# Performance work log

Hardware: AMD Instinct MI355X
Metric: run time of the kernel (lower is better)

## Reference

```python
import jax, jax.numpy as jnp
import numpy as np

B, N, K = 8, 2048, 100  # graphs per batch, nodes per graph, diffpool clusters


def _bn(x, g, b, eps=1e-5):
    # BatchNorm1d in training mode over all B*N nodes (biased variance)
    m = x.mean(axis=(0, 1))
    v = x.var(axis=(0, 1))
    return (x - m) * jax.lax.rsqrt(v + eps) * g + b


def _norm_adj(A):
    # PyG gcn_norm: add remaining self-loops (fill=1), D^-1/2 (A+I) D^-1/2
    n = A.shape[-1]
    d = jnp.diagonal(A, axis1=-2, axis2=-1)
    A_hat = A + jnp.where(d == 0, 1.0, 0.0)[..., :, None] * jnp.eye(n, dtype=A.dtype)
    deg = A_hat.sum(-1)
    dinv = jnp.where(deg > 0, 1.0 / jnp.sqrt(deg), 0.0)
    return dinv[..., :, None] * A_hat * dinv[..., None, :]


def _gcn(An, x, W, b):
    # GCNConv: propagate(x @ W) + bias, with pre-normalized adjacency
    return An @ (x @ W) + b


def _forward(x, adj, W_in, W3030, Wp13, b30, b100, Wfc_pool, bfc_pool,
             W1, b1, W2, b2, gamma30, beta30, gamma100, beta100):
    A_w = _norm_adj(adj)                               # weighted (edge_attr) adjacency
    A_b = _norm_adj((adj > 0).astype(adj.dtype))       # pool convs ignore edge_attr
    # feature branch
    x11 = _bn(_gcn(A_w, x, W_in[0], b30[0]), gamma30[0], beta30[0])
    x12 = _bn(_gcn(A_w, x11, W3030[0], b30[1]), gamma30[1], beta30[1])
    x13 = _bn(_gcn(A_w, x12, W3030[1], b30[2]), gamma30[2], beta30[2])
    x1_out = jnp.concatenate([x11, x12, x13], -1).max(axis=1)   # [B,90]
    # assignment branch
    s11 = _bn(_gcn(A_b, x, W_in[1], b30[3]), gamma30[3], beta30[3])
    s12 = _bn(_gcn(A_b, s11, W3030[2], b30[4]), gamma30[4], beta30[4])
    s13 = _bn(_gcn(A_b, s12, Wp13, b100), gamma100, beta100)
    s1 = jnp.concatenate([s11, s12, s13], -1) @ Wfc_pool + bfc_pool  # [B,N,K]
    # dense_diff_pool (link/entropy losses are unused by the forward output)
    s = jax.nn.softmax(s1, -1)
    p1_x = jnp.einsum('bnk,bnd->bkd', s, x13)          # s^T x  [B,K,30]
    p1_adj = jnp.einsum('bnk,bnl->bkl', s, adj @ s)    # s^T A s  [B,K,K]
    # second stage on pooled (dense, weighted) graph
    A2 = _norm_adj(p1_adj)
    x21 = _bn(_gcn(A2, p1_x, W3030[3], b30[5]), gamma30[5], beta30[5])
    x22 = _bn(_gcn(A2, x21, W3030[4], b30[6]), gamma30[6], beta30[6])
    x23 = _bn(_gcn(A2, x22, W3030[5], b30[7]), gamma30[7], beta30[7])
    x2_out = jnp.concatenate([x21, x22, x23], -1).max(axis=1)   # [B,90]
    h = jnp.concatenate([x1_out, x2_out], -1) @ W1 + b1
    return jax.nn.relu(h) @ W2 + b2                    # [B,6]


def setup_inputs():
    key = jax.random.key(0)
    ks = jax.random.split(key, 12)
    u = jax.random.uniform(ks[0], (B, N, N), dtype=jnp.float32)
    mask = jax.random.uniform(ks[1], (B, N, N)) < 0.05
    A = jnp.triu(u * mask, 1)
    adj = A + jnp.swapaxes(A, -1, -2)
    x = jax.random.normal(ks[2], (B, N, 3), dtype=jnp.float32)
    w = lambda k, s: jax.random.normal(k, s, dtype=jnp.float32) * 0.1
    return dict(
        x=x, adj=adj,
        W_in=w(ks[3], (2, 3, 30)),      # conv11, pool_conv11
        W3030=w(ks[4], (6, 30, 30)),    # conv12, conv13, pool_conv12, conv21..23
        Wp13=w(ks[5], (30, 100)),
        b30=jnp.zeros((8, 30), jnp.float32),
        b100=jnp.zeros((100,), jnp.float32),
        Wfc_pool=w(ks[6], (160, 100)), bfc_pool=jnp.zeros((100,), jnp.float32),
        W1=w(ks[7], (180, 50)), b1=jnp.zeros((50,), jnp.float32),
        W2=w(ks[8], (50, 6)), b2=jnp.zeros((6,), jnp.float32),
        gamma30=jnp.ones((8, 30), jnp.float32), beta30=jnp.zeros((8, 30), jnp.float32),
        gamma100=jnp.ones((100,), jnp.float32), beta100=jnp.zeros((100,), jnp.float32),
    )


def reference(x, adj, W_in, W3030, Wp13, b30, b100, Wfc_pool, bfc_pool,
              W1, b1, W2, b2, gamma30, beta30, gamma100, beta100):
    return _forward(x, adj, W_in, W3030, Wp13, b30, b100, Wfc_pool, bfc_pool,
                    W1, b1, W2, b2, gamma30, beta30, gamma100, beta100)
```

## Files before the change

kernel.cpp:

```cpp
#include <hip/hip_runtime.h>
#include <hip/hip_fp16.h>
#include <cstdint>
#include <cstddef>

#define BATCH 8
#define NN 2048
#define RTOT 16384
#define CAP 176

static constexpr size_t OF_B1W   = 0;
static constexpr size_t OF_B1B   = 3840;
static constexpr size_t OF_B2W   = 7680;
static constexpr size_t OF_B2B   = 11520;
static constexpr size_t OF_B3W   = 15360;
static constexpr size_t OF_B3B   = 15840;
static constexpr size_t OF_S2    = 17440;
static constexpr size_t OF_CNT   = 17620;
static constexpr size_t ZEND     = 17632;
static constexpr size_t OF_ELLV  = 17664;
static constexpr size_t OF_ELLC  = OF_ELLV + 2883584;
static constexpr size_t OF_ROWLEN= OF_ELLC + 1441792;
static constexpr size_t OF_DINVW = OF_ROWLEN + 16384;
static constexpr size_t OF_DINVB = OF_DINVW + 16384;
static constexpr size_t OF_HWB   = OF_DINVB + 16384;
static constexpr size_t OF_HW3   = OF_HWB + 524288;
static constexpr size_t OF_HB100 = OF_HW3 + 262144;
static constexpr size_t OF_ZW    = OF_HB100 + 851968;
static constexpr size_t OF_ZB    = OF_ZW + 524288;
static constexpr size_t OF_X11   = OF_ZB + 1703936;
static constexpr size_t OF_X12   = OF_X11 + 524288;
static constexpr size_t OF_X13   = OF_X12 + 524288;
static constexpr size_t OF_S11   = OF_X13 + 524288;
static constexpr size_t OF_S12   = OF_S11 + 524288;
static constexpr size_t OF_PARTMAX = OF_S12 + 524288;

#define FMA4(acc, s, h) { acc.x += (s)*(h).x; acc.y += (s)*(h).y; acc.z += (s)*(h).z; acc.w += (s)*(h).w; }

__device__ __forceinline__ unsigned short f2h(float f) {
  _Float16 h = (_Float16)f;
  return *(unsigned short*)&h;
}
__device__ __forceinline__ float h2f(unsigned short s) {
  _Float16 h = *(_Float16*)&s;
  return (float)h;
}
__device__ __forceinline__ float2 h2f2(unsigned int u) {
  __half2 h = *(__half2*)&u;
  return __half22float2(h);
}

struct __align__(8) us4 { unsigned short x, y, z, w; };

#define ACC8(g, wt) { \
  float2 f0=h2f2((g).x), f1=h2f2((g).y), f2=h2f2((g).z), f3=h2f2((g).w); \
  acc[0] += (wt)*f0.x; acc[1] += (wt)*f0.y; acc[2] += (wt)*f1.x; acc[3] += (wt)*f1.y; \
  acc[4] += (wt)*f2.x; acc[5] += (wt)*f2.y; acc[6] += (wt)*f3.x; acc[7] += (wt)*f3.y; }


__global__ __launch_bounds__(256) void k_build_ell(
    const float* __restrict__ adj, const float* __restrict__ x,
    const float* __restrict__ Win, float* __restrict__ ellv,
    unsigned short* __restrict__ ellc, int* __restrict__ rowlen,
    float* __restrict__ dinvw, float* __restrict__ dinvb,
    unsigned short* __restrict__ Hwb, float* __restrict__ zbase)
{
  int r = blockIdx.x;
  int t = threadIdx.x, lane = t & 63, wv = t >> 6;
  if (blockIdx.x < 69) {
    int zi = blockIdx.x * 256 + t;
    if (zi < (int)ZEND) zbase[zi] = 0.f;
  }
  const float* row = adj + (size_t)r * NN;
  __shared__ int wcnt[4];
  __shared__ float wsumA[4];
  __shared__ float dsh[2];
  float4 a = ((const float4*)row)[t];
  float4 b = ((const float4*)row)[256 + t];
  float vals[8] = {a.x, a.y, a.z, a.w, b.x, b.y, b.z, b.w};
  int cbase0 = t*4, cbase1 = 1024 + t*4;
  int cnt = 0; float sum = 0.f;
#pragma unroll
  for (int k = 0; k < 8; ++k) { sum += vals[k]; cnt += (vals[k] != 0.f) ? 1 : 0; }
  int pre = cnt;
#pragma unroll
  for (int o = 1; o < 64; o <<= 1) { int n = __shfl_up(pre, o); if (lane >= o) pre += n; }
  int excl = pre - cnt;
  int wtot = __shfl(pre, 63);
#pragma unroll
  for (int o = 32; o; o >>= 1) sum += __shfl_down(sum, o);
  if (lane == 0) { wcnt[wv] = wtot; wsumA[wv] = sum; }
  __syncthreads();
  int base = 0;
  for (int w = 0; w < wv; ++w) base += wcnt[w];
  int p = base + excl;
  size_t rb = (size_t)r * CAP;
#pragma unroll
  for (int k = 0; k < 8; ++k) {
    float v = vals[k];
    if (v != 0.f && p < CAP) {
      ellv[rb + p] = v;
      ellc[rb + p] = (unsigned short)((k < 4) ? (cbase0 + k) : (cbase1 + (k - 4)));
      ++p;
    }
  }
  if (t == 0) {
    int tot = wcnt[0] + wcnt[1] + wcnt[2] + wcnt[3];
    float ws = wsumA[0] + wsumA[1] + wsumA[2] + wsumA[3];
    int nnz = tot < CAP ? tot : CAP;
    int n = nnz;
    while ((n & 3) && n < CAP) { ellv[rb + n] = 0.f; ellc[rb + n] = 0; ++n; }
    rowlen[r] = n;
    float dw = rsqrtf(ws + 1.f), db = rsqrtf((float)nnz + 1.f);
    dinvw[r] = dw; dinvb[r] = db;
    dsh[0] = dw; dsh[1] = db;
  }
  __syncthreads();
  if (t < 64) {
    int c = t & 31, side = t >> 5;
    float v = 0.f;
    if (c < 30) {
      float x0 = x[r*3], x1 = x[r*3+1], x2 = x[r*3+2];
      const float* W = Win + side*90;
      v = (x0*W[c] + x1*W[30+c] + x2*W[60+c]) * dsh[side];
    }
    Hwb[(size_t)r*64 + t] = f2h(v);
  }
}

__global__ __launch_bounds__(256) void k_spmm_pair(
    const unsigned short* __restrict__ Hwb, const float* __restrict__ ellv,
    const unsigned short* __restrict__ ellc, const int* __restrict__ rowlen,
    const float* __restrict__ dinvw, const float* __restrict__ dinvb,
    float* __restrict__ Zw, float* __restrict__ Zb,
    float* __restrict__ bktW, float* __restrict__ bktB)
{
  __shared__ float zsW[32][32];
  __shared__ float zsB[32][32];
  int t = threadIdx.x;
  int gid = blockIdx.x * 256 + t;
  int row = gid >> 3, q = gid & 7;
  int side = q >> 2, sub = q & 3;
  int len = rowlen[row];
  const float4* ev = (const float4*)(ellv + (size_t)row * CAP);
  const uint2*  ec = (const uint2*) (ellc + (size_t)row * CAP);
  const uint4* HP = (const uint4*)(Hwb + (size_t)(row >> 11) * (NN*64));
  float acc[8] = {0,0,0,0,0,0,0,0};
  int nit = len >> 2;
  for (int i = 0; i < nit; ++i) {
    float4 v = ev[i];
    uint2 cc = ec[i];
    int c0 = cc.x & 0xffff, c1 = cc.x >> 16, c2 = cc.y & 0xffff, c3 = cc.y >> 16;
    uint4 g0 = HP[c0*8+q], g1 = HP[c1*8+q], g2 = HP[c2*8+q], g3 = HP[c3*8+q];
    float w0 = side ? (v.x>0.f?1.f:0.f) : v.x;
    float w1 = side ? (v.y>0.f?1.f:0.f) : v.y;
    float w2 = side ? (v.z>0.f?1.f:0.f) : v.z;
    float w3 = side ? (v.w>0.f?1.f:0.f) : v.w;
    ACC8(g0, w0); ACC8(g1, w1); ACC8(g2, w2); ACC8(g3, w3);
  }
  uint4 hs = HP[(row & (NN-1))*8 + q];
  ACC8(hs, 1.f);
  float d = side ? dinvb[row] : dinvw[row];
#pragma unroll
  for (int k = 0; k < 8; ++k) acc[k] *= d;
  float* Zp = (side ? Zb : Zw) + (size_t)row*32 + sub*8;
  float4 o0 = {acc[0],acc[1],acc[2],acc[3]}, o1 = {acc[4],acc[5],acc[6],acc[7]};
  ((float4*)Zp)[0] = o0; ((float4*)Zp)[1] = o1;
  int rowloc = t >> 3;
  float (*zs)[32] = side ? zsB : zsW;
#pragma unroll
  for (int k = 0; k < 8; ++k) zs[rowloc][sub*8+k] = acc[k];
  __syncthreads();
  int copy = blockIdx.x & 63;
  if (t < 30) {
    float s1 = 0.f, s2 = 0.f;
    for (int r = 0; r < 32; ++r) { float v = zsW[r][t]; s1 += v; s2 += v*v; }
    atomicAdd(&bktW[(t*64+copy)*2],   s1);
    atomicAdd(&bktW[(t*64+copy)*2+1], s2);
  } else if (t >= 64 && t < 94) {
    int c = t - 64;
    float s1 = 0.f, s2 = 0.f;
    for (int r = 0; r < 32; ++r) { float v = zsB[r][c]; s1 += v; s2 += v*v; }
    atomicAdd(&bktB[(c*64+copy)*2],   s1);
    atomicAdd(&bktB[(c*64+copy)*2+1], s2);
  }
}

__global__ __launch_bounds__(256) void k_spmm_l3(
    const unsigned short* __restrict__ Hw3, const unsigned short* __restrict__ Hb100,
    const float* __restrict__ ellv, const unsigned short* __restrict__ ellc,
    const int* __restrict__ rowlen, const float* __restrict__ dinvw,
    const float* __restrict__ dinvb, float* __restrict__ Zw, float* __restrict__ Zb,
    float* __restrict__ bktW3, float* __restrict__ bktB3)
{
  __shared__ float zs[64][32];
  __shared__ float st[200];
  int t = threadIdx.x;
  if (blockIdx.x < 256) {
    int gid = blockIdx.x * 256 + t;
    int row = gid >> 2, q = gid & 3;
    int len = rowlen[row];
    const float4* ev = (const float4*)(ellv + (size_t)row * CAP);
    const uint2*  ec = (const uint2*) (ellc + (size_t)row * CAP);
    const uint4* HP = (const uint4*)(Hw3 + (size_t)(row >> 11) * (NN*32));
    float acc[8] = {0,0,0,0,0,0,0,0};
    int nit = len >> 2;
    for (int i = 0; i < nit; ++i) {
      float4 v = ev[i];
      uint2 cc = ec[i];
      int c0 = cc.x & 0xffff, c1 = cc.x >> 16, c2 = cc.y & 0xffff, c3 = cc.y >> 16;
      uint4 g0 = HP[c0*4+q], g1 = HP[c1*4+q], g2 = HP[c2*4+q], g3 = HP[c3*4+q];
      ACC8(g0, v.x); ACC8(g1, v.y); ACC8(g2, v.z); ACC8(g3, v.w);
    }
    uint4 hs = HP[(row & (NN-1))*4 + q];
    ACC8(hs, 1.f);
    float d = dinvw[row];
#pragma unroll
    for (int k = 0; k < 8; ++k) acc[k] *= d;
    float* Zp = Zw + (size_t)row*32 + q*8;
    float4 o0 = {acc[0],acc[1],acc[2],acc[3]}, o1 = {acc[4],acc[5],acc[6],acc[7]};
    ((float4*)Zp)[0] = o0; ((float4*)Zp)[1] = o1;
    int rowloc = t >> 2;
#pragma unroll
    for (int k = 0; k < 8; ++k) zs[rowloc][q*8+k] = acc[k];
    __syncthreads();
    if (t < 30) {
      float s1 = 0.f, s2 = 0.f;
      for (int r = 0; r < 64; ++r) { float v = zs[r][t]; s1 += v; s2 += v*v; }
      int copy = blockIdx.x & 7;
      atomicAdd(&bktW3[(t*8+copy)*2],   s1);
      atomicAdd(&bktW3[(t*8+copy)*2+1], s2);
    }
  } else {
    int bid = blockIdx.x - 256;
    for (int i = t; i < 200; i += 256) st[i] = 0.f;
    __syncthreads();
    int gid = bid * 256 + t;
    int row = gid / 13, q = gid - row*13;
    int len = rowlen[row];
    const float4* ev = (const float4*)(ellv + (size_t)row * CAP);
    const uint2*  ec = (const uint2*) (ellc + (size_t)row * CAP);
    const uint4* HP = (const uint4*)(Hb100 + (size_t)(row >> 11) * ((size_t)NN*104));
    float acc[8] = {0,0,0,0,0,0,0,0};
    int nit = len >> 2;
    for (int i = 0; i < nit; ++i) {
      float4 v = ev[i];
      uint2 cc = ec[i];
      int c0 = cc.x & 0xffff, c1 = cc.x >> 16, c2 = cc.y & 0xffff, c3 = cc.y >> 16;
      uint4 g0 = HP[c0*13+q], g1 = HP[c1*13+q], g2 = HP[c2*13+q], g3 = HP[c3*13+q];
      float w0 = (v.x>0.f?1.f:0.f), w1 = (v.y>0.f?1.f:0.f);
      float w2 = (v.z>0.f?1.f:0.f), w3 = (v.w>0.f?1.f:0.f);
      ACC8(g0, w0); ACC8(g1, w1); ACC8(g2, w2); ACC8(g3, w3);
    }
    uint4 hs = HP[(row & (NN-1))*13 + q];
    ACC8(hs, 1.f);
    float d = dinvb[row];
#pragma unroll
    for (int k = 0; k < 8; ++k) acc[k] *= d;
    float* Zp = Zb + (size_t)row*104 + q*8;
    float4 o0 = {acc[0],acc[1],acc[2],acc[3]}, o1 = {acc[4],acc[5],acc[6],acc[7]};
    ((float4*)Zp)[0] = o0; ((float4*)Zp)[1] = o1;
    int c0 = q*8;
#pragma unroll
    for (int k = 0; k < 8; ++k) {
      int ch = c0 + k;
      if (ch < 100) { atomicAdd(&st[ch*2], acc[k]); atomicAdd(&st[ch*2+1], acc[k]*acc[k]); }
    }
    __syncthreads();
    int copy = bid & 7;
    for (int i = t; i < 200; i += 256)
      atomicAdd(&bktB3[((i>>1)*8 + copy)*2 + (i&1)], st[i]);
  }
}

template<int LEVEL>
__global__ __launch_bounds__(256) void k_apply_gemm(
    const float* __restrict__ Zw, const float* __restrict__ bktW,
    const float* __restrict__ gW, const float* __restrict__ beW,
    float* __restrict__ xst, const float* __restrict__ Ww,
    const float* __restrict__ dinvw,
    const float* __restrict__ Zb, const float* __restrict__ bktB,
    const float* __restrict__ gB, const float* __restrict__ beB,
    float* __restrict__ sst, const float* __restrict__ Wb,
    const float* __restrict__ dinvb,
    unsigned short* __restrict__ HwOut, unsigned short* __restrict__ HbOut)
{
  constexpr int NGB = (LEVEL == 1) ? 8 : 26;
  constexpr int OSTRIDEB = (LEVEL == 1) ? 32 : 104;
  constexpr int NG = 8 + NGB;
  __shared__ float WwL[30*32];
  __shared__ float WbL[30*OSTRIDEB];
  __shared__ float awL[60], abL[60];
  int t = threadIdx.x;
  if (t < 60) {
    int c = t % 30;
    bool isW = t < 30;
    const float4* p = (const float4*)((isW ? bktW : bktB) + c*128);
    float s1 = 0.f, s2 = 0.f;
#pragma unroll
    for (int k = 0; k < 32; ++k) { float4 v = p[k]; s1 += v.x + v.z; s2 += v.y + v.w; }
    float mean = s1/16384.f, var = s2/16384.f - mean*mean, inv = rsqrtf(var + 1e-5f);
    float aa = (isW ? gW : gB)[c]*inv;
    float* dst = isW ? awL : abL;
    dst[c] = aa; dst[30+c] = (isW ? beW : beB)[c] - mean*aa;
  }
  for (int idx = t; idx < 30*32; idx += 256) {
    int k = idx >> 5, c = idx & 31;
    WwL[idx] = (c < 30) ? Ww[k*30 + c] : 0.f;
  }
  if (LEVEL == 1) {
    for (int idx = t; idx < 30*32; idx += 256) {
      int k = idx >> 5, c = idx & 31;
      WbL[idx] = (c < 30) ? Wb[k*30 + c] : 0.f;
    }
  } else {
    for (int idx = t; idx < 30*OSTRIDEB; idx += 256) {
      int k = idx / OSTRIDEB, j = idx % OSTRIDEB;
      WbL[idx] = (j < 100) ? Wb[k*100 + j] : 0.f;
    }
  }
  __syncthreads();
  int gid = blockIdx.x * 256 + t;
  int row = gid / NG, g = gid % NG;
  if (g < 8) {
    const float4* Z4 = (const float4*)Zw + (size_t)row*8;
    float4 z4[8];
#pragma unroll
    for (int u = 0; u < 8; ++u) z4[u] = Z4[u];
    const float* z = (const float*)z4;
    float4 xv;
    int ch = 4*g;
    xv.x = (ch+0 < 30) ? awL[ch+0]*z[ch+0] + awL[30+ch+0] : 0.f;
    xv.y = (ch+1 < 30) ? awL[ch+1]*z[ch+1] + awL[30+ch+1] : 0.f;
    xv.z = (ch+2 < 30) ? awL[ch+2]*z[ch+2] + awL[30+ch+2] : 0.f;
    xv.w = (ch+3 < 30) ? awL[ch+3]*z[ch+3] + awL[30+ch+3] : 0.f;
    ((float4*)xst)[(size_t)row*8+g] = xv;
    float4 o = {0,0,0,0};
#pragma unroll
    for (int k = 0; k < 30; ++k) {
      float xk = awL[k]*z[k] + awL[30+k];
      float4 w = *(const float4*)(WwL + k*32 + 4*g);
      FMA4(o, xk, w);
    }
    float d = dinvw[row];
    us4 pv = { f2h(d*o.x), f2h(d*o.y), f2h(d*o.z), f2h(d*o.w) };
    unsigned short* dst = (LEVEL == 1) ? (HwOut + (size_t)row*64 + 4*g)
                                       : (HwOut + (size_t)row*32 + 4*g);
    *(us4*)dst = pv;
  } else {
    int gb = g - 8;
    const float4* Z4 = (const float4*)Zb + (size_t)row*8;
    float4 z4[8];
#pragma unroll
    for (int u = 0; u < 8; ++u) z4[u] = Z4[u];
    const float* z = (const float*)z4;
    if (gb < 8) {
      int ch = 4*gb;
      float4 sv;
      sv.x = (ch+0 < 30) ? abL[ch+0]*z[ch+0] + abL[30+ch+0] : 0.f;
      sv.y = (ch+1 < 30) ? abL[ch+1]*z[ch+1] + abL[30+ch+1] : 0.f;
      sv.z = (ch+2 < 30) ? abL[ch+2]*z[ch+2] + abL[30+ch+2] : 0.f;
      sv.w = (ch+3 < 30) ? abL[ch+3]*z[ch+3] + abL[30+ch+3] : 0.f;
      ((float4*)sst)[(size_t)row*8+gb] = sv;
    }
    float4 o = {0,0,0,0};
#pragma unroll
    for (int k = 0; k < 30; ++k) {
      float sk = abL[k]*z[k] + abL[30+k];
      float4 w = *(const float4*)(WbL + k*OSTRIDEB + 4*gb);
      FMA4(o, sk, w);
    }
    float d = dinvb[row];
    us4 pv = { f2h(d*o.x), f2h(d*o.y), f2h(d*o.z), f2h(d*o.w) };
    unsigned short* dst = (LEVEL == 1) ? (HbOut + (size_t)row*64 + 32 + 4*gb)
                                       : (HbOut + (size_t)row*104 + 4*gb);
    *(us4*)dst = pv;
  }
}

__global__ __launch_bounds__(256) void k_fcpool(
    const float* __restrict__ Zw3, const float* __restrict__ bktW3,
    const float* __restrict__ gW3, const float* __restrict__ beW3,
    const float* __restrict__ Zb3, const float* __restrict__ bktB3,
    const float* __restrict__ g100, const float* __restrict__ be100,
    const float* __restrict__ s11, const float* __restrict__ s12,
    const float* __restrict__ Wfc, const float* __restrict__ bfc,
    float* __restrict__ x13, unsigned short* __restrict__ S)
{
  __shared__ float shm[14240];
  __shared__ float aw3[60], ab3[200];
  float* feat = shm;
  float* Wl = shm + 10240;
  int t = threadIdx.x;
  int g0 = blockIdx.x * 64;
  if (t < 30) {
    const float4* p = (const float4*)(bktW3 + t*16);
    float s1 = 0.f, s2 = 0.f;
#pragma unroll
    for (int k = 0; k < 4; ++k) { float4 v = p[k]; s1 += v.x + v.z; s2 += v.y + v.w; }
    float mean = s1/16384.f, var = s2/16384.f - mean*mean, inv = rsqrtf(var + 1e-5f);
    float aa = gW3[t]*inv; aw3[t] = aa; aw3[30+t] = beW3[t] - mean*aa;
  } else if (t >= 64 && t < 164) {
    int c = t - 64;
    const float4* p = (const float4*)(bktB3 + c*16);
    float s1 = 0.f, s2 = 0.f;
#pragma unroll
    for (int k = 0; k < 4; ++k) { float4 v = p[k]; s1 += v.x + v.z; s2 += v.y + v.w; }
    float mean = s1/16384.f, var = s2/16384.f - mean*mean, inv = rsqrtf(var + 1e-5f);
    float aa = g100[c]*inv; ab3[c] = aa; ab3[100+c] = be100[c] - mean*aa;
  }
  __syncthreads();
  for (int idx = t; idx < 64*160; idx += 256) {
    int l = idx / 160, c = idx % 160;
    int g = g0 + l;
    float v;
    if (c < 30) v = s11[(size_t)g*32 + c];
    else if (c < 60) v = s12[(size_t)g*32 + (c-30)];
    else { int k = c - 60; v = ab3[k]*Zb3[(size_t)g*104 + k] + ab3[100 + k]; }
    feat[l*160 + c] = v;
  }
  for (int idx = t; idx < 64*32; idx += 256) {
    int l = idx >> 5, c = idx & 31;
    int g = g0 + l;
    x13[(size_t)g*32+c] = (c < 30) ? aw3[c]*Zw3[(size_t)g*32+c] + aw3[30+c] : 0.f;
  }
  int np = t >> 3, kg = t & 7;
  int n0 = np*2, n1 = np*2 + 1;
  int kbase = kg*12 + (kg < 4 ? kg : 4);
  int klen  = kg < 4 ? 13 : 12;
  float a0[13], a1[13];
#pragma unroll
  for (int j = 0; j < 13; ++j) { a0[j] = 0.f; a1[j] = 0.f; }
  for (int ch = 0; ch < 4; ++ch) {
    __syncthreads();
    for (int idx = t; idx < 4000; idx += 256) {
      int r = idx/100, j = idx%100;
      Wl[r*100 + j] = Wfc[(ch*40 + r)*100 + j];
    }
    __syncthreads();
    for (int kk = 0; kk < 40; ++kk) {
      float f0 = feat[n0*160 + ch*40+kk];
      float f1 = feat[n1*160 + ch*40+kk];
#pragma unroll
      for (int j = 0; j < 13; ++j) {
        if (j < klen) {
          float w = Wl[kk*100 + kbase + j];
          a0[j] += f0*w; a1[j] += f1*w;
        }
      }
    }
  }
  __syncthreads();
  float* sRow = shm;
  for (int j = 0; j < klen; ++j) {
    int k = kbase + j;
    sRow[n0*100 + k] = a0[j] + bfc[k];
    sRow[n1*100 + k] = a1[j] + bfc[k];
  }
  __syncthreads();
  int n = t >> 2, part = t & 3;
  int i0 = part*25;
  float m = -3.4e38f;
  for (int i = 0; i < 25; ++i) m = fmaxf(m, sRow[n*100 + i0 + i]);
  m = fmaxf(m, __shfl_xor(m, 1));
  m = fmaxf(m, __shfl_xor(m, 2));
  float ev[25]; float s = 0.f;
  for (int i = 0; i < 25; ++i) { float e = __expf(sRow[n*100 + i0 + i] - m); ev[i] = e; s += e; }
  s += __shfl_xor(s, 1);
  s += __shfl_xor(s, 2);
  float rinv = 1.f / s;
  for (int i = 0; i < 25; ++i) S[(size_t)(g0+n)*104 + i0 + i] = f2h(ev[i] * rinv);
  if (part == 3) {
    S[(size_t)(g0+n)*104 + 100] = 0; S[(size_t)(g0+n)*104 + 101] = 0;
    S[(size_t)(g0+n)*104 + 102] = 0; S[(size_t)(g0+n)*104 + 103] = 0;
  }
}

__global__ __launch_bounds__(256) void k_spmm_as(
    const unsigned short* __restrict__ S, const float* __restrict__ ellv,
    const unsigned short* __restrict__ ellc, const int* __restrict__ rowlen,
    float* __restrict__ Z)
{
  int t = threadIdx.x;
  int gid = blockIdx.x * 256 + t;
  int row = gid / 13, q = gid - row*13;
  int len = rowlen[row];
  const float4* ev = (const float4*)(ellv + (size_t)row * CAP);
  const uint2*  ec = (const uint2*) (ellc + (size_t)row * CAP);
  const uint4* HP = (const uint4*)(S + (size_t)(row >> 11) * ((size_t)NN*104));
  float acc[8] = {0,0,0,0,0,0,0,0};
  int nit = len >> 2;
  for (int i = 0; i < nit; ++i) {
    float4 v = ev[i];
    uint2 cc = ec[i];
    int c0 = cc.x & 0xffff, c1 = cc.x >> 16, c2 = cc.y & 0xffff, c3 = cc.y >> 16;
    uint4 g0 = HP[c0*13+q], g1 = HP[c1*13+q], g2 = HP[c2*13+q], g3 = HP[c3*13+q];
    ACC8(g0, v.x); ACC8(g1, v.y); ACC8(g2, v.z); ACC8(g3, v.w);
  }
  float* Zp = Z + (size_t)row*104 + q*8;
  float4 o0 = {acc[0],acc[1],acc[2],acc[3]}, o1 = {acc[4],acc[5],acc[6],acc[7]};
  ((float4*)Zp)[0] = o0; ((float4*)Zp)[1] = o1;
}

__global__ __launch_bounds__(256) void k_pool_part(
    const unsigned short* __restrict__ S, const float* __restrict__ x13,
    const float* __restrict__ As, const float* __restrict__ x11,
    const float* __restrict__ x12, float* __restrict__ pp, float* __restrict__ pm)
{
  __shared__ float sL[64][100];
  __shared__ float xL[64][132];
  __shared__ float red[256];
  int t = threadIdx.x;
  int b = blockIdx.x >> 3, chunk = blockIdx.x & 7;
  int g00 = b * 2048 + chunk * 256;
  int kt = t/10, dt = t%10;
  int k0 = kt*4, d0 = dt*13;
  float acc[4][13];
#pragma unroll
  for (int a = 0; a < 4; ++a)
#pragma unroll
    for (int j = 0; j < 13; ++j) acc[a][j] = 0.f;
  for (int tile = 0; tile < 4; ++tile) {
    int g0 = g00 + tile*64;
    __syncthreads();
    for (int idx = t; idx < 64*100; idx += 256) {
      int l = idx/100, k = idx%100;
      sL[l][k] = h2f(S[(size_t)(g0+l)*104 + k]);
    }
    for (int idx = t; idx < 64*130; idx += 256) {
      int l = idx/130, d = idx%130;
      xL[l][d] = d < 30 ? x13[(size_t)(g0+l)*32 + d] : As[(size_t)(g0+l)*104 + (d-30)];
    }
    __syncthreads();
    if (t < 250) {
      for (int kk = 0; kk < 64; ++kk) {
        float sv[4];
#pragma unroll
        for (int a = 0; a < 4; ++a) sv[a] = sL[kk][k0+a];
#pragma unroll
        for (int j = 0; j < 13; ++j) {
          float xv = xL[kk][d0+j];
#pragma unroll
          for (int a = 0; a < 4; ++a) acc[a][j] += sv[a]*xv;
        }
      }
    }
  }
  if (t < 250) {
    float* dst = pp + (size_t)blockIdx.x * 13000;
    for (int a = 0; a < 4; ++a)
      for (int j = 0; j < 13; ++j)
        dst[(k0+a)*130 + (d0+j)] = acc[a][j];
  }
  __syncthreads();
  {
    int c = t & 31, rg = t >> 5;
    const float* srcs[3] = {x11, x12, x13};
    for (int a = 0; a < 3; ++a) {
      const float* p = srcs[a] + (size_t)(g00+rg)*32 + c;
      float m = -3.4e38f;
      for (int it = 0; it < 32; ++it) m = fmaxf(m, p[it*256]);
      red[t] = m;
      __syncthreads();
      if (t < 30) {
        float mm = red[t];
        for (int g = 1; g < 8; ++g) mm = fmaxf(mm, red[g*32+t]);
        pm[(size_t)blockIdx.x*90 + a*30 + t] = mm;
      }
      __syncthreads();
    }
  }
}

__global__ __launch_bounds__(256) void k_s2fused(
    const float* __restrict__ pp, const float* __restrict__ partmax,
    const float* __restrict__ Wm,
    const float* __restrict__ g30,
    const float* __restrict__ be30,
    float* __restrict__ bktS2,
    int* __restrict__ cnt,
    const float* __restrict__ W1, const float* __restrict__ b1,
    const float* __restrict__ W2, const float* __restrict__ b2,
    float* __restrict__ out)
{
  __shared__ float A2f[10000];
  __shared__ float buf1[3000];
  __shared__ float buf2[3200];
  __shared__ float WL[960];
  __shared__ float dl[100];
  __shared__ float st1[30], st2[30];
  __shared__ float coef[60];
  __shared__ float x1L[90], x2L[90], hh[50];
  int b = blockIdx.x, t = threadIdx.x;
  for (int idx = t; idx < 13000; idx += 256) {
    float s = 0.f;
    for (int ch = 0; ch < 8; ++ch) s += pp[(size_t)(b*8 + ch)*13000 + idx];
    int k = idx/130, d = idx%130;
    if (d < 30) buf1[k*30 + d] = s;
    else A2f[k*100 + (d-30)] = s;
  }
  __syncthreads();
  if (t < 100 && A2f[t*101] == 0.f) A2f[t*101] = 1.f;
  __syncthreads();
  if (t < 100) {
    float s = 0.f;
    for (int j = 0; j < 100; ++j) s += A2f[t*100 + j];
    dl[t] = s > 0.f ? rsqrtf(s) : 0.f;
  }
  __syncthreads();
  for (int idx = t; idx < 10000; idx += 256) {
    int i = idx/100, j = idx%100;
    A2f[idx] = dl[i]*dl[j]*A2f[idx];
  }
  int rp = t >> 2, cg = t & 3;
  int i0 = rp*2, c0 = cg*8;
  bool act = (t < 200);
  for (int L = 0; L < 3; ++L) {
    if (t < 30) { st1[t] = 0.f; st2[t] = 0.f; }
    const float* W = Wm + L*900;
    for (int idx = t; idx < 960; idx += 256) {
      int k = idx >> 5, c = idx & 31;
      WL[idx] = (c < 30) ? W[k*30 + c] : 0.f;
    }
    __syncthreads();
    if (act) {
      float a0[8] = {0,0,0,0,0,0,0,0}, a1[8] = {0,0,0,0,0,0,0,0};
      for (int k = 0; k < 30; ++k) {
        float xx0 = buf1[i0*30 + k], xx1 = buf1[(i0+1)*30 + k];
        float4 w0 = *(const float4*)&WL[k*32 + c0];
        float4 w1 = *(const float4*)&WL[k*32 + c0 + 4];
        a0[0] += xx0*w0.x; a0[1] += xx0*w0.y; a0[2] += xx0*w0.z; a0[3] += xx0*w0.w;
        a0[4] += xx0*w1.x; a0[5] += xx0*w1.y; a0[6] += xx0*w1.z; a0[7] += xx0*w1.w;
        a1[0] += xx1*w0.x; a1[1] += xx1*w0.y; a1[2] += xx1*w0.z; a1[3] += xx1*w0.w;
        a1[4] += xx1*w1.x; a1[5] += xx1*w1.y; a1[6] += xx1*w1.z; a1[7] += xx1*w1.w;
      }
      float4 s00 = {a0[0],a0[1],a0[2],a0[3]}, s01 = {a0[4],a0[5],a0[6],a0[7]};
      float4 s10 = {a1[0],a1[1],a1[2],a1[3]}, s11v = {a1[4],a1[5],a1[6],a1[7]};
      *(float4*)&buf2[i0*32 + c0]       = s00;
      *(float4*)&buf2[i0*32 + c0 + 4]   = s01;
      *(float4*)&buf2[(i0+1)*32 + c0]   = s10;
      *(float4*)&buf2[(i0+1)*32 + c0+4] = s11v;
    }
    __syncthreads();
    if (act) {
      float z0[8] = {0,0,0,0,0,0,0,0}, z1[8] = {0,0,0,0,0,0,0,0};
      for (int j = 0; j < 100; ++j) {
        float av0 = A2f[i0*100 + j], av1 = A2f[(i0+1)*100 + j];
        float4 t0 = *(const float4*)&buf2[j*32 + c0];
        float4 t1 = *(const float4*)&buf2[j*32 + c0 + 4];
        z0[0] += av0*t0.x; z0[1] += av0*t0.y; z0[2] += av0*t0.z; z0[3] += av0*t0.w;
        z0[4] += av0*t1.x; z0[5] += av0*t1.y; z0[6] += av0*t1.z; z0[7] += av0*t1.w;
        z1[0] += av1*t0.x; z1[1] += av1*t0.y; z1[2] += av1*t0.z; z1[3] += av1*t0.w;
        z1[4] += av1*t1.x; z1[5] += av1*t1.y; z1[6] += av1*t1.z; z1[7] += av1*t1.w;
      }
#pragma unroll
      for (int k = 0; k < 8; ++k) {
        int c = c0 + k;
        if (c < 30) {
          buf1[i0*30 + c]     = z0[k];
          buf1[(i0+1)*30 + c] = z1[k];
          atomicAdd(&st1[c], z0[k] + z1[k]);
          atomicAdd(&st2[c], z0[k]*z0[k] + z1[k]*z1[k]);
        }
      }
    }
    __syncthreads();
    if (t < 30) {
      atomicAdd(&bktS2[(L*30+t)*2],   st1[t]);
      atomicAdd(&bktS2[(L*30+t)*2+1], st2[t]);
    }
    __syncthreads();
    if (t == 0) {
      __threadfence();
      atomicAdd(cnt, 1);
      while (atomicAdd(cnt, 0) < (L+1)*8) {}
      __threadfence();
    }
    __syncthreads();
    if (t < 30) {
      float s1 = atomicAdd(&bktS2[(L*30+t)*2],   0.f);
      float s2 = atomicAdd(&bktS2[(L*30+t)*2+1], 0.f);
      float mean = s1/800.f, var = s2/800.f - mean*mean, inv = rsqrtf(var + 1e-5f);
      float aa = g30[L*30+t]*inv;
      coef[t] = aa; coef[30+t] = be30[L*30+t] - mean*aa;
    }
    __syncthreads();
    if (L < 2) {
      for (int idx = t; idx < 3000; idx += 256) {
        int c = idx % 30;
        buf1[idx] = coef[c]*buf1[idx] + coef[30+c];
      }
      __syncthreads();
      if (t < 30) {
        float m = -3.4e38f;
        for (int i = 0; i < 100; ++i) m = fmaxf(m, buf1[i*30+t]);
        x2L[L*30+t] = m;
      }
      __syncthreads();
    } else {
      if (t < 30) {
        float m = -3.4e38f;
        for (int i = 0; i < 100; ++i) m = fmaxf(m, coef[t]*buf1[i*30+t] + coef[30+t]);
        x2L[60+t] = m;
      }
    }
  }
  if (t < 90) {
    float m = -3.4e38f;
    for (int s = 0; s < 8; ++s) m = fmaxf(m, partmax[(size_t)(b*8+s)*90 + t]);
    x1L[t] = m;
  }
  __syncthreads();
  if (t < 50) {
    float a = b1[t];
    for (int k = 0; k < 90; ++k) a += x1L[k]*W1[k*50+t];
    for (int k = 0; k < 90; ++k) a += x2L[k]*W1[(90+k)*50+t];
    hh[t] = fmaxf(a, 0.f);
  }
  __syncthreads();
  if (t < 6) {
    float a = b2[t];
    for (int j = 0; j < 50; ++j) a += hh[j]*W2[j*6+t];
    out[b*6+t] = a;
  }
}

extern "C" void kernel_launch(void* const* d_in, const int* in_sizes, int n_in,
                              void* d_out, int out_size, void* d_ws, size_t ws_size,
                              hipStream_t stream)
{
  const float* x    = (const float*)d_in[0];
  const float* adj  = (const float*)d_in[1];
  const float* Win  = (const float*)d_in[2];
  const float* W3030= (const float*)d_in[3];
  const float* Wp13 = (const float*)d_in[4];
  const float* Wfc  = (const float*)d_in[7];
  const float* bfc  = (const float*)d_in[8];
  const float* W1   = (const float*)d_in[9];
  const float* b1   = (const float*)d_in[10];
  const float* W2   = (const float*)d_in[11];
  const float* b2   = (const float*)d_in[12];
  const float* g30  = (const float*)d_in[13];
  const float* be30 = (const float*)d_in[14];
  const float* g100 = (const float*)d_in[15];
  const float* be100= (const float*)d_in[16];
  float* out = (float*)d_out;

  float* wsf = (float*)d_ws;
  float* bL1W = wsf + OF_B1W;  float* bL1B = wsf + OF_B1B;
  float* bL2W = wsf + OF_B2W;  float* bL2B = wsf + OF_B2B;
  float* bL3W = wsf + OF_B3W;  float* bL3B = wsf + OF_B3B;
  float* bktS2 = wsf + OF_S2;
  int*   cnt  = (int*)(wsf + OF_CNT);
  float* ellv  = wsf + OF_ELLV;
  unsigned short* ellc = (unsigned short*)(wsf + OF_ELLC);
  int*   rowlen = (int*)(wsf + OF_ROWLEN);
  float* dinvw = wsf + OF_DINVW;
  float* dinvb = wsf + OF_DINVB;
  unsigned short* Hwb   = (unsigned short*)(wsf + OF_HWB);
  unsigned short* Hw3   = (unsigned short*)(wsf + OF_HW3);
  unsigned short* Hb100 = (unsigned short*)(wsf + OF_HB100);
  unsigned short* S     = Hb100;
  float* Zw = wsf + OF_ZW;
  float* Zb = wsf + OF_ZB;
  float* x11 = wsf + OF_X11;
  float* x12 = wsf + OF_X12;
  float* x13 = wsf + OF_X13;
  float* s11 = wsf + OF_S11;
  float* s12 = wsf + OF_S12;
  float* pp  = wsf + OF_S11;
  float* partmax = wsf + OF_PARTMAX;

  k_build_ell<<<RTOT, 256, 0, stream>>>(adj, x, Win, ellv, ellc, rowlen, dinvw, dinvb, Hwb, wsf);

  k_spmm_pair<<<512, 256, 0, stream>>>(Hwb, ellv, ellc, rowlen, dinvw, dinvb, Zw, Zb, bL1W, bL1B);
  k_apply_gemm<1><<<1024, 256, 0, stream>>>(Zw, bL1W, g30+0, be30+0, x11, W3030+0, dinvw,
                                            Zb, bL1B, g30+90, be30+90, s11, W3030+2*900, dinvb, Hwb, Hwb);

  k_spmm_pair<<<512, 256, 0, stream>>>(Hwb, ellv, ellc, rowlen, dinvw, dinvb, Zw, Zb, bL2W, bL2B);
  k_apply_gemm<2><<<2176, 256, 0, stream>>>(Zw, bL2W, g30+30, be30+30, x12, W3030+900, dinvw,
                                            Zb, bL2B, g30+120, be30+120, s12, Wp13, dinvb, Hw3, Hb100);

  k_spmm_l3<<<1088, 256, 0, stream>>>(Hw3, Hb100, ellv, ellc, rowlen, dinvw, dinvb, Zw, Zb, bL3W, bL3B);
  k_fcpool<<<256, 256, 0, stream>>>(Zw, bL3W, g30+60, be30+60, Zb, bL3B, g100, be100,
                                    s11, s12, Wfc, bfc, x13, S);

  k_spmm_as<<<832, 256, 0, stream>>>(S, ellv, ellc, rowlen, Zb );
  k_pool_part<<<64, 256, 0, stream>>>(S, x13, Zb, x11, x12, pp, partmax);

  k_s2fused<<<BATCH, 256, 0, stream>>>(pp, partmax, W3030+3*900, g30+150, be30+150,
                                       bktS2, cnt, W1, b1, W2, b2, out);
}
```

Measured before the change: 655.8 us.

## Fuse all stages into one persistent kernel with software grid barriers

Replaces the sequence of nine kernel launches with a single persistent kernel of 512 blocks that steps through every stage and separates them with atomic-counter grid barriers. Intermediate buffers are given separate workspace regions so phases no longer alias each other, and the zeroing of the counters and accumulators moves to a hipMemsetAsync. The aim is to remove launch gaps and per-kernel tail effects. In exchange, each stage runs with a fixed grid and 256 threads per block, so occupancy and parallelism per stage change, the barriers spin on global atomics, and the large static shared array may limit how many blocks fit per CU. Correctness relies on all 512 blocks being resident at the same time.

```diff
diff --git a/kernel.cpp b/kernel.cpp
--- a/kernel.cpp
+++ b/kernel.cpp
@@ -7,6 +7,7 @@
 #define NN 2048
 #define RTOT 16384
 #define CAP 176
+#define NBLK 512
 
 static constexpr size_t OF_B1W   = 0;
 static constexpr size_t OF_B1B   = 3840;
@@ -22,17 +23,25 @@
 static constexpr size_t OF_ROWLEN= OF_ELLC + 1441792;
 static constexpr size_t OF_DINVW = OF_ROWLEN + 16384;
 static constexpr size_t OF_DINVB = OF_DINVW + 16384;
-static constexpr size_t OF_HWB   = OF_DINVB + 16384;
-static constexpr size_t OF_HW3   = OF_HWB + 524288;
+static constexpr size_t OF_HWB1  = OF_DINVB + 16384;
+static constexpr size_t OF_HWB2  = OF_HWB1 + 524288;
+static constexpr size_t OF_HW3   = OF_HWB2 + 524288;
 static constexpr size_t OF_HB100 = OF_HW3 + 262144;
-static constexpr size_t OF_ZW    = OF_HB100 + 851968;
-static constexpr size_t OF_ZB    = OF_ZW + 524288;
-static constexpr size_t OF_X11   = OF_ZB + 1703936;
+static constexpr size_t OF_S     = OF_HB100 + 851968;
+static constexpr size_t OF_ZWA   = OF_S + 851968;
+static constexpr size_t OF_ZBA   = OF_ZWA + 524288;
+static constexpr size_t OF_ZWB   = OF_ZBA + 524288;
+static constexpr size_t OF_ZBB   = OF_ZWB + 524288;
+static constexpr size_t OF_ZWC   = OF_ZBB + 524288;
+static constexpr size_t OF_ZBC   = OF_ZWC + 524288;
+static constexpr size_t OF_AS    = OF_ZBC + 1703936;
+static constexpr size_t OF_X11   = OF_AS + 1703936;
 static constexpr size_t OF_X12   = OF_X11 + 524288;
 static constexpr size_t OF_X13   = OF_X12 + 524288;
 static constexpr size_t OF_S11   = OF_X13 + 524288;
 static constexpr size_t OF_S12   = OF_S11 + 524288;
-static constexpr size_t OF_PARTMAX = OF_S12 + 524288;
+static constexpr size_t OF_PP    = OF_S12 + 524288;
+static constexpr size_t OF_PARTMAX = OF_PP + 832000;
 
 #define FMA4(acc, s, h) { acc.x += (s)*(h).x; acc.y += (s)*(h).y; acc.z += (s)*(h).z; acc.w += (s)*(h).w; }
 
@@ -56,88 +65,26 @@
   acc[0] += (wt)*f0.x; acc[1] += (wt)*f0.y; acc[2] += (wt)*f1.x; acc[3] += (wt)*f1.y; \
   acc[4] += (wt)*f2.x; acc[5] += (wt)*f2.y; acc[6] += (wt)*f3.x; acc[7] += (wt)*f3.y; }
 
-
-__global__ __launch_bounds__(256) void k_build_ell(
-    const float* __restrict__ adj, const float* __restrict__ x,
-    const float* __restrict__ Win, float* __restrict__ ellv,
-    unsigned short* __restrict__ ellc, int* __restrict__ rowlen,
-    float* __restrict__ dinvw, float* __restrict__ dinvb,
-    unsigned short* __restrict__ Hwb, float* __restrict__ zbase)
+__device__ __forceinline__ void gridbar(int* cnt, int target) {
+  __syncthreads();
+  if (threadIdx.x == 0) {
+    __threadfence();
+    atomicAdd(cnt, 1);
+    while (atomicAdd(cnt, 0) < target) {}
+    __threadfence();
+  }
+  __syncthreads();
+}
+
+__device__ __forceinline__ void spmm_pair_body(
+    int vb, int t, float* shm,
+    const unsigned short* Hwb, const float* ellv, const unsigned short* ellc,
+    const int* rowlen, const float* dinvw, const float* dinvb,
+    float* Zw, float* Zb, float* bktW, float* bktB)
 {
-  int r = blockIdx.x;
-  int t = threadIdx.x, lane = t & 63, wv = t >> 6;
-  if (blockIdx.x < 69) {
-    int zi = blockIdx.x * 256 + t;
-    if (zi < (int)ZEND) zbase[zi] = 0.f;
-  }
-  const float* row = adj + (size_t)r * NN;
-  __shared__ int wcnt[4];
-  __shared__ float wsumA[4];
-  __shared__ float dsh[2];
-  float4 a = ((const float4*)row)[t];
-  float4 b = ((const float4*)row)[256 + t];
-  float vals[8] = {a.x, a.y, a.z, a.w, b.x, b.y, b.z, b.w};
-  int cbase0 = t*4, cbase1 = 1024 + t*4;
-  int cnt = 0; float sum = 0.f;
-#pragma unroll
-  for (int k = 0; k < 8; ++k) { sum += vals[k]; cnt += (vals[k] != 0.f) ? 1 : 0; }
-  int pre = cnt;
-#pragma unroll
-  for (int o = 1; o < 64; o <<= 1) { int n = __shfl_up(pre, o); if (lane >= o) pre += n; }
-  int excl = pre - cnt;
-  int wtot = __shfl(pre, 63);
-#pragma unroll
-  for (int o = 32; o; o >>= 1) sum += __shfl_down(sum, o);
-  if (lane == 0) { wcnt[wv] = wtot; wsumA[wv] = sum; }
-  __syncthreads();
-  int base = 0;
-  for (int w = 0; w < wv; ++w) base += wcnt[w];
-  int p = base + excl;
-  size_t rb = (size_t)r * CAP;
-#pragma unroll
-  for (int k = 0; k < 8; ++k) {
-    float v = vals[k];
-    if (v != 0.f && p < CAP) {
-      ellv[rb + p] = v;
-      ellc[rb + p] = (unsigned short)((k < 4) ? (cbase0 + k) : (cbase1 + (k - 4)));
-      ++p;
-    }
-  }
-  if (t == 0) {
-    int tot = wcnt[0] + wcnt[1] + wcnt[2] + wcnt[3];
-    float ws = wsumA[0] + wsumA[1] + wsumA[2] + wsumA[3];
-    int nnz = tot < CAP ? tot : CAP;
-    int n = nnz;
-    while ((n & 3) && n < CAP) { ellv[rb + n] = 0.f; ellc[rb + n] = 0; ++n; }
-    rowlen[r] = n;
-    float dw = rsqrtf(ws + 1.f), db = rsqrtf((float)nnz + 1.f);
-    dinvw[r] = dw; dinvb[r] = db;
-    dsh[0] = dw; dsh[1] = db;
-  }
-  __syncthreads();
-  if (t < 64) {
-    int c = t & 31, side = t >> 5;
-    float v = 0.f;
-    if (c < 30) {
-      float x0 = x[r*3], x1 = x[r*3+1], x2 = x[r*3+2];
-      const float* W = Win + side*90;
-      v = (x0*W[c] + x1*W[30+c] + x2*W[60+c]) * dsh[side];
-    }
-    Hwb[(size_t)r*64 + t] = f2h(v);
-  }
-}
-
-__global__ __launch_bounds__(256) void k_spmm_pair(
-    const unsigned short* __restrict__ Hwb, const float* __restrict__ ellv,
-    const unsigned short* __restrict__ ellc, const int* __restrict__ rowlen,
-    const float* __restrict__ dinvw, const float* __restrict__ dinvb,
-    float* __restrict__ Zw, float* __restrict__ Zb,
-    float* __restrict__ bktW, float* __restrict__ bktB)
-{
-  __shared__ float zsW[32][32];
-  __shared__ float zsB[32][32];
-  int t = threadIdx.x;
-  int gid = blockIdx.x * 256 + t;
+  float* zsW = shm;
+  float* zsB = shm + 1024;
+  int gid = vb * 256 + t;
   int row = gid >> 3, q = gid & 7;
   int side = q >> 2, sub = q & 3;
   int len = rowlen[row];
@@ -166,80 +113,419 @@
   float4 o0 = {acc[0],acc[1],acc[2],acc[3]}, o1 = {acc[4],acc[5],acc[6],acc[7]};
   ((float4*)Zp)[0] = o0; ((float4*)Zp)[1] = o1;
   int rowloc = t >> 3;
-  float (*zs)[32] = side ? zsB : zsW;
-#pragma unroll
-  for (int k = 0; k < 8; ++k) zs[rowloc][sub*8+k] = acc[k];
+  float* zs = side ? zsB : zsW;
+#pragma unroll
+  for (int k = 0; k < 8; ++k) zs[rowloc*32 + sub*8+k] = acc[k];
   __syncthreads();
-  int copy = blockIdx.x & 63;
+  int copy = vb & 63;
   if (t < 30) {
     float s1 = 0.f, s2 = 0.f;
-    for (int r = 0; r < 32; ++r) { float v = zsW[r][t]; s1 += v; s2 += v*v; }
+    for (int r = 0; r < 32; ++r) { float v = zsW[r*32 + t]; s1 += v; s2 += v*v; }
     atomicAdd(&bktW[(t*64+copy)*2],   s1);
     atomicAdd(&bktW[(t*64+copy)*2+1], s2);
   } else if (t >= 64 && t < 94) {
     int c = t - 64;
     float s1 = 0.f, s2 = 0.f;
-    for (int r = 0; r < 32; ++r) { float v = zsB[r][c]; s1 += v; s2 += v*v; }
+    for (int r = 0; r < 32; ++r) { float v = zsB[r*32 + c]; s1 += v; s2 += v*v; }
     atomicAdd(&bktB[(c*64+copy)*2],   s1);
     atomicAdd(&bktB[(c*64+copy)*2+1], s2);
   }
 }
 
-__global__ __launch_bounds__(256) void k_spmm_l3(
-    const unsigned short* __restrict__ Hw3, const unsigned short* __restrict__ Hb100,
-    const float* __restrict__ ellv, const unsigned short* __restrict__ ellc,
-    const int* __restrict__ rowlen, const float* __restrict__ dinvw,
-    const float* __restrict__ dinvb, float* __restrict__ Zw, float* __restrict__ Zb,
-    float* __restrict__ bktW3, float* __restrict__ bktB3)
+template<int LEVEL>
+__device__ __forceinline__ void apply_phase(
+    int blk, int t, float* shm,
+    const float* Zw, const float* bktW, const float* gW, const float* beW,
+    float* xst, const float* Ww, const float* dinvw,
+    const float* Zb, const float* bktB, const float* gB, const float* beB,
+    float* sst, const float* Wb, const float* dinvb,
+    unsigned short* HwOut, unsigned short* HbOut)
 {
-  __shared__ float zs[64][32];
-  __shared__ float st[200];
-  int t = threadIdx.x;
-  if (blockIdx.x < 256) {
-    int gid = blockIdx.x * 256 + t;
-    int row = gid >> 2, q = gid & 3;
-    int len = rowlen[row];
-    const float4* ev = (const float4*)(ellv + (size_t)row * CAP);
-    const uint2*  ec = (const uint2*) (ellc + (size_t)row * CAP);
-    const uint4* HP = (const uint4*)(Hw3 + (size_t)(row >> 11) * (NN*32));
-    float acc[8] = {0,0,0,0,0,0,0,0};
-    int nit = len >> 2;
-    for (int i = 0; i < nit; ++i) {
-      float4 v = ev[i];
-      uint2 cc = ec[i];
-      int c0 = cc.x & 0xffff, c1 = cc.x >> 16, c2 = cc.y & 0xffff, c3 = cc.y >> 16;
-      uint4 g0 = HP[c0*4+q], g1 = HP[c1*4+q], g2 = HP[c2*4+q], g3 = HP[c3*4+q];
-      ACC8(g0, v.x); ACC8(g1, v.y); ACC8(g2, v.z); ACC8(g3, v.w);
-    }
-    uint4 hs = HP[(row & (NN-1))*4 + q];
-    ACC8(hs, 1.f);
-    float d = dinvw[row];
-#pragma unroll
-    for (int k = 0; k < 8; ++k) acc[k] *= d;
-    float* Zp = Zw + (size_t)row*32 + q*8;
-    float4 o0 = {acc[0],acc[1],acc[2],acc[3]}, o1 = {acc[4],acc[5],acc[6],acc[7]};
-    ((float4*)Zp)[0] = o0; ((float4*)Zp)[1] = o1;
-    int rowloc = t >> 2;
-#pragma unroll
-    for (int k = 0; k < 8; ++k) zs[rowloc][q*8+k] = acc[k];
-    __syncthreads();
+  constexpr int NGB = (LEVEL == 1) ? 8 : 26;
+  constexpr int OSTRIDEB = (LEVEL == 1) ? 32 : 104;
+  constexpr int NG = 8 + NGB;
+  constexpr int NVB = RTOT * NG / 256;
+  float* WwL = shm;
+  float* WbL = shm + 960;
+  float* awL = shm + 4080;
+  float* abL = shm + 4140;
+  if (t < 60) {
+    int c = t % 30;
+    bool isW = t < 30;
+    const float4* p = (const float4*)((isW ? bktW : bktB) + c*128);
+    float s1 = 0.f, s2 = 0.f;
+#pragma unroll
+    for (int k = 0; k < 32; ++k) { float4 v = p[k]; s1 += v.x + v.z; s2 += v.y + v.w; }
+    float mean = s1/16384.f, var = s2/16384.f - mean*mean, inv = rsqrtf(var + 1e-5f);
+    float aa = (isW ? gW : gB)[c]*inv;
+    float* dst = isW ? awL : abL;
+    dst[c] = aa; dst[30+c] = (isW ? beW : beB)[c] - mean*aa;
+  }
+  for (int idx = t; idx < 30*32; idx += 256) {
+    int k = idx >> 5, c = idx & 31;
+    WwL[idx] = (c < 30) ? Ww[k*30 + c] : 0.f;
+  }
+  if (LEVEL == 1) {
+    for (int idx = t; idx < 30*32; idx += 256) {
+      int k = idx >> 5, c = idx & 31;
+      WbL[idx] = (c < 30) ? Wb[k*30 + c] : 0.f;
+    }
+  } else {
+    for (int idx = t; idx < 30*OSTRIDEB; idx += 256) {
+      int k = idx / OSTRIDEB, j = idx % OSTRIDEB;
+      WbL[idx] = (j < 100) ? Wb[k*100 + j] : 0.f;
+    }
+  }
+  __syncthreads();
+  for (int vb = blk; vb < NVB; vb += NBLK) {
+    int gid = vb * 256 + t;
+    int row = gid / NG, g = gid % NG;
+    if (g < 8) {
+      const float4* Z4 = (const float4*)Zw + (size_t)row*8;
+      float4 z4[8];
+#pragma unroll
+      for (int u = 0; u < 8; ++u) z4[u] = Z4[u];
+      const float* z = (const float*)z4;
+      float4 xv;
+      int ch = 4*g;
+      xv.x = (ch+0 < 30) ? awL[ch+0]*z[ch+0] + awL[30+ch+0] : 0.f;
+      xv.y = (ch+1 < 30) ? awL[ch+1]*z[ch+1] + awL[30+ch+1] : 0.f;
+      xv.z = (ch+2 < 30) ? awL[ch+2]*z[ch+2] + awL[30+ch+2] : 0.f;
+      xv.w = (ch+3 < 30) ? awL[ch+3]*z[ch+3] + awL[30+ch+3] : 0.f;
+      ((float4*)xst)[(size_t)row*8+g] = xv;
+      float4 o = {0,0,0,0};
+#pragma unroll
+      for (int k = 0; k < 30; ++k) {
+        float xk = awL[k]*z[k] + awL[30+k];
+        float4 w = *(const float4*)(WwL + k*32 + 4*g);
+        FMA4(o, xk, w);
+      }
+      float d = dinvw[row];
+      us4 pv = { f2h(d*o.x), f2h(d*o.y), f2h(d*o.z), f2h(d*o.w) };
+      unsigned short* dst = (LEVEL == 1) ? (HwOut + (size_t)row*64 + 4*g)
+                                         : (HwOut + (size_t)row*32 + 4*g);
+      *(us4*)dst = pv;
+    } else {
+      int gb = g - 8;
+      const float4* Z4 = (const float4*)Zb + (size_t)row*8;
+      float4 z4[8];
+#pragma unroll
+      for (int u = 0; u < 8; ++u) z4[u] = Z4[u];
+      const float* z = (const float*)z4;
+      if (gb < 8) {
+        int ch = 4*gb;
+        float4 sv;
+        sv.x = (ch+0 < 30) ? abL[ch+0]*z[ch+0] + abL[30+ch+0] : 0.f;
+        sv.y = (ch+1 < 30) ? abL[ch+1]*z[ch+1] + abL[30+ch+1] : 0.f;
+        sv.z = (ch+2 < 30) ? abL[ch+2]*z[ch+2] + abL[30+ch+2] : 0.f;
+        sv.w = (ch+3 < 30) ? abL[ch+3]*z[ch+3] + abL[30+ch+3] : 0.f;
+        ((float4*)sst)[(size_t)row*8+gb] = sv;
+      }
+      float4 o = {0,0,0,0};
+#pragma unroll
+      for (int k = 0; k < 30; ++k) {
+        float sk = abL[k]*z[k] + abL[30+k];
+        float4 w = *(const float4*)(WbL + k*OSTRIDEB + 4*gb);
+        FMA4(o, sk, w);
+      }
+      float d = dinvb[row];
+      us4 pv = { f2h(d*o.x), f2h(d*o.y), f2h(d*o.z), f2h(d*o.w) };
+      unsigned short* dst = (LEVEL == 1) ? (HbOut + (size_t)row*64 + 32 + 4*gb)
+                                         : (HbOut + (size_t)row*104 + 4*gb);
+      *(us4*)dst = pv;
+    }
+  }
+}
+
+__global__ __launch_bounds__(256) void k_mega(
+    const float* adj, const float* x, const float* Win, const float* W3030,
+    const float* Wp13, const float* Wfc, const float* bfc,
+    const float* W1, const float* b1, const float* W2, const float* b2,
+    const float* g30, const float* be30, const float* g100, const float* be100,
+    float* wsf, float* out)
+{
+  __shared__ float shm[17664];
+  const int blk = blockIdx.x, t = threadIdx.x;
+  int* cnt  = (int*)(wsf + OF_CNT);
+  int* cnt2 = cnt + 1;
+  float* ellv = wsf + OF_ELLV;
+  unsigned short* ellc = (unsigned short*)(wsf + OF_ELLC);
+  int* rowlen = (int*)(wsf + OF_ROWLEN);
+  float* dinvw = wsf + OF_DINVW;
+  float* dinvb = wsf + OF_DINVB;
+  unsigned short* Hwb1 = (unsigned short*)(wsf + OF_HWB1);
+  unsigned short* Hwb2 = (unsigned short*)(wsf + OF_HWB2);
+  unsigned short* Hw3  = (unsigned short*)(wsf + OF_HW3);
+  unsigned short* Hb100= (unsigned short*)(wsf + OF_HB100);
+  unsigned short* S    = (unsigned short*)(wsf + OF_S);
+  float* ZwA = wsf + OF_ZWA;  float* ZbA = wsf + OF_ZBA;
+  float* ZwB = wsf + OF_ZWB;  float* ZbB = wsf + OF_ZBB;
+  float* ZwC = wsf + OF_ZWC;  float* ZbC = wsf + OF_ZBC;
+  float* As  = wsf + OF_AS;
+  float* x11 = wsf + OF_X11;  float* x12 = wsf + OF_X12;  float* x13 = wsf + OF_X13;
+  float* s11 = wsf + OF_S11;  float* s12 = wsf + OF_S12;
+  float* pp  = wsf + OF_PP;   float* partmax = wsf + OF_PARTMAX;
+  float* bL1W = wsf + OF_B1W;  float* bL1B = wsf + OF_B1B;
+  float* bL2W = wsf + OF_B2W;  float* bL2B = wsf + OF_B2B;
+  float* bL3W = wsf + OF_B3W;  float* bL3B = wsf + OF_B3B;
+  float* bktS2 = wsf + OF_S2;
+
+  {
+    int* wcnt = (int*)shm;
+    float* wsumA = shm + 4;
+    float* dsh = shm + 8;
+    int lane = t & 63, wv = t >> 6;
+    for (int r = blk; r < RTOT; r += NBLK) {
+      __syncthreads();
+      const float* row = adj + (size_t)r * NN;
+      float4 a = ((const float4*)row)[t];
+      float4 b = ((const float4*)row)[256 + t];
+      float vals[8] = {a.x, a.y, a.z, a.w, b.x, b.y, b.z, b.w};
+      int cbase0 = t*4, cbase1 = 1024 + t*4;
+      int cnt_ = 0; float sum = 0.f;
+#pragma unroll
+      for (int k = 0; k < 8; ++k) { sum += vals[k]; cnt_ += (vals[k] != 0.f) ? 1 : 0; }
+      int pre = cnt_;
+#pragma unroll
+      for (int o = 1; o < 64; o <<= 1) { int n = __shfl_up(pre, o); if (lane >= o) pre += n; }
+      int excl = pre - cnt_;
+      int wtot = __shfl(pre, 63);
+#pragma unroll
+      for (int o = 32; o; o >>= 1) sum += __shfl_down(sum, o);
+      if (lane == 0) { wcnt[wv] = wtot; wsumA[wv] = sum; }
+      __syncthreads();
+      int base = 0;
+      for (int w = 0; w < wv; ++w) base += wcnt[w];
+      int p = base + excl;
+      size_t rb = (size_t)r * CAP;
+#pragma unroll
+      for (int k = 0; k < 8; ++k) {
+        float v = vals[k];
+        if (v != 0.f && p < CAP) {
+          ellv[rb + p] = v;
+          ellc[rb + p] = (unsigned short)((k < 4) ? (cbase0 + k) : (cbase1 + (k - 4)));
+          ++p;
+        }
+      }
+      if (t == 0) {
+        int tot = wcnt[0] + wcnt[1] + wcnt[2] + wcnt[3];
+        float ws = wsumA[0] + wsumA[1] + wsumA[2] + wsumA[3];
+        int nnz = tot < CAP ? tot : CAP;
+        int n = nnz;
+        while ((n & 3) && n < CAP) { ellv[rb + n] = 0.f; ellc[rb + n] = 0; ++n; }
+        rowlen[r] = n;
+        float dw = rsqrtf(ws + 1.f), db = rsqrtf((float)nnz + 1.f);
+        dinvw[r] = dw; dinvb[r] = db;
+        dsh[0] = dw; dsh[1] = db;
+      }
+      __syncthreads();
+      if (t < 64) {
+        int c = t & 31, side = t >> 5;
+        float v = 0.f;
+        if (c < 30) {
+          float x0 = x[r*3], x1 = x[r*3+1], x2 = x[r*3+2];
+          const float* W = Win + side*90;
+          v = (x0*W[c] + x1*W[30+c] + x2*W[60+c]) * dsh[side];
+        }
+        Hwb1[(size_t)r*64 + t] = f2h(v);
+      }
+    }
+  }
+  gridbar(cnt, 1*NBLK);
+
+  spmm_pair_body(blk, t, shm, Hwb1, ellv, ellc, rowlen, dinvw, dinvb, ZwA, ZbA, bL1W, bL1B);
+  gridbar(cnt, 2*NBLK);
+
+  apply_phase<1>(blk, t, shm, ZwA, bL1W, g30+0, be30+0, x11, W3030+0, dinvw,
+                 ZbA, bL1B, g30+90, be30+90, s11, W3030+2*900, dinvb, Hwb2, Hwb2);
+  gridbar(cnt, 3*NBLK);
+
+  spmm_pair_body(blk, t, shm, Hwb2, ellv, ellc, rowlen, dinvw, dinvb, ZwB, ZbB, bL2W, bL2B);
+  gridbar(cnt, 4*NBLK);
+
+  apply_phase<2>(blk, t, shm, ZwB, bL2W, g30+30, be30+30, x12, W3030+900, dinvw,
+                 ZbB, bL2B, g30+120, be30+120, s12, Wp13, dinvb, Hw3, Hb100);
+  gridbar(cnt, 5*NBLK);
+
+  for (int vb = blk; vb < 1088; vb += NBLK) {
+    __syncthreads();
+    if (vb < 256) {
+      float* zs = shm;
+      int gid = vb * 256 + t;
+      int row = gid >> 2, q = gid & 3;
+      int len = rowlen[row];
+      const float4* ev = (const float4*)(ellv + (size_t)row * CAP);
+      const uint2*  ec = (const uint2*) (ellc + (size_t)row * CAP);
+      const uint4* HP = (const uint4*)(Hw3 + (size_t)(row >> 11) * (NN*32));
+      float acc[8] = {0,0,0,0,0,0,0,0};
+      int nit = len >> 2;
+      for (int i = 0; i < nit; ++i) {
+        float4 v = ev[i];
+        uint2 cc = ec[i];
+        int c0 = cc.x & 0xffff, c1 = cc.x >> 16, c2 = cc.y & 0xffff, c3 = cc.y >> 16;
+        uint4 g0 = HP[c0*4+q], g1 = HP[c1*4+q], g2 = HP[c2*4+q], g3 = HP[c3*4+q];
+        ACC8(g0, v.x); ACC8(g1, v.y); ACC8(g2, v.z); ACC8(g3, v.w);
+      }
+      uint4 hs = HP[(row & (NN-1))*4 + q];
+      ACC8(hs, 1.f);
+      float d = dinvw[row];
+#pragma unroll
+      for (int k = 0; k < 8; ++k) acc[k] *= d;
+      float* Zp = ZwC + (size_t)row*32 + q*8;
+      float4 o0 = {acc[0],acc[1],acc[2],acc[3]}, o1 = {acc[4],acc[5],acc[6],acc[7]};
+      ((float4*)Zp)[0] = o0; ((float4*)Zp)[1] = o1;
+      int rowloc = t >> 2;
+#pragma unroll
+      for (int k = 0; k < 8; ++k) zs[rowloc*32 + q*8+k] = acc[k];
+      __syncthreads();
+      if (t < 30) {
+        float s1 = 0.f, s2 = 0.f;
+        for (int r = 0; r < 64; ++r) { float v = zs[r*32 + t]; s1 += v; s2 += v*v; }
+        int copy = vb & 7;
+        atomicAdd(&bL3W[(t*8+copy)*2],   s1);
+        atomicAdd(&bL3W[(t*8+copy)*2+1], s2);
+      }
+    } else {
+      float* st = shm + 2048;
+      int bid = vb - 256;
+      for (int i = t; i < 200; i += 256) st[i] = 0.f;
+      __syncthreads();
+      int gid = bid * 256 + t;
+      int row = gid / 13, q = gid - row*13;
+      int len = rowlen[row];
+      const float4* ev = (const float4*)(ellv + (size_t)row * CAP);
+      const uint2*  ec = (const uint2*) (ellc + (size_t)row * CAP);
+      const uint4* HP = (const uint4*)(Hb100 + (size_t)(row >> 11) * ((size_t)NN*104));
+      float acc[8] = {0,0,0,0,0,0,0,0};
+      int nit = len >> 2;
+      for (int i = 0; i < nit; ++i) {
+        float4 v = ev[i];
+        uint2 cc = ec[i];
+        int c0 = cc.x & 0xffff, c1 = cc.x >> 16, c2 = cc.y & 0xffff, c3 = cc.y >> 16;
+        uint4 g0 = HP[c0*13+q], g1 = HP[c1*13+q], g2 = HP[c2*13+q], g3 = HP[c3*13+q];
+        float w0 = (v.x>0.f?1.f:0.f), w1 = (v.y>0.f?1.f:0.f);
+        float w2 = (v.z>0.f?1.f:0.f), w3 = (v.w>0.f?1.f:0.f);
+        ACC8(g0, w0); ACC8(g1, w1); ACC8(g2, w2); ACC8(g3, w3);
+      }
+      uint4 hs = HP[(row & (NN-1))*13 + q];
+      ACC8(hs, 1.f);
+      float d = dinvb[row];
+#pragma unroll
+      for (int k = 0; k < 8; ++k) acc[k] *= d;
+      float* Zp = ZbC + (size_t)row*104 + q*8;
+      float4 o0 = {acc[0],acc[1],acc[2],acc[3]}, o1 = {acc[4],acc[5],acc[6],acc[7]};
+      ((float4*)Zp)[0] = o0; ((float4*)Zp)[1] = o1;
+      int c0 = q*8;
+#pragma unroll
+      for (int k = 0; k < 8; ++k) {
+        int ch = c0 + k;
+        if (ch < 100) { atomicAdd(&st[ch*2], acc[k]); atomicAdd(&st[ch*2+1], acc[k]*acc[k]); }
+      }
+      __syncthreads();
+      int copy = bid & 7;
+      for (int i = t; i < 200; i += 256)
+        atomicAdd(&bL3B[((i>>1)*8 + copy)*2 + (i&1)], st[i]);
+    }
+  }
+  gridbar(cnt, 6*NBLK);
+
+  if (blk < 256) {
+    float* feat = shm;
+    float* Wl = shm + 10240;
+    float* aw3 = shm + 14240;
+    float* ab3 = shm + 14300;
+    int g0 = blk * 64;
     if (t < 30) {
+      const float4* p = (const float4*)(bL3W + t*16);
       float s1 = 0.f, s2 = 0.f;
-      for (int r = 0; r < 64; ++r) { float v = zs[r][t]; s1 += v; s2 += v*v; }
-      int copy = blockIdx.x & 7;
-      atomicAdd(&bktW3[(t*8+copy)*2],   s1);
-      atomicAdd(&bktW3[(t*8+copy)*2+1], s2);
-    }
-  } else {
-    int bid = blockIdx.x - 256;
-    for (int i = t; i < 200; i += 256) st[i] = 0.f;
-    __syncthreads();
-    int gid = bid * 256 + t;
+#pragma unroll
+      for (int k = 0; k < 4; ++k) { float4 v = p[k]; s1 += v.x + v.z; s2 += v.y + v.w; }
+      float mean = s1/16384.f, var = s2/16384.f - mean*mean, inv = rsqrtf(var + 1e-5f);
+      float aa = g30[60+t]*inv; aw3[t] = aa; aw3[30+t] = be30[60+t] - mean*aa;
+    } else if (t >= 64 && t < 164) {
+      int c = t - 64;
+      const float4* p = (const float4*)(bL3B + c*16);
+      float s1 = 0.f, s2 = 0.f;
+#pragma unroll
+      for (int k = 0; k < 4; ++k) { float4 v = p[k]; s1 += v.x + v.z; s2 += v.y + v.w; }
+      float mean = s1/16384.f, var = s2/16384.f - mean*mean, inv = rsqrtf(var + 1e-5f);
+      float aa = g100[c]*inv; ab3[c] = aa; ab3[100+c] = be100[c] - mean*aa;
+    }
+    __syncthreads();
+    for (int idx = t; idx < 64*160; idx += 256) {
+      int l = idx / 160, c = idx % 160;
+      int g = g0 + l;
+      float v;
+      if (c < 30) v = s11[(size_t)g*32 + c];
+      else if (c < 60) v = s12[(size_t)g*32 + (c-30)];
+      else { int k = c - 60; v = ab3[k]*ZbC[(size_t)g*104 + k] + ab3[100 + k]; }
+      feat[l*160 + c] = v;
+    }
+    for (int idx = t; idx < 64*32; idx += 256) {
+      int l = idx >> 5, c = idx & 31;
+      int g = g0 + l;
+      x13[(size_t)g*32+c] = (c < 30) ? aw3[c]*ZwC[(size_t)g*32+c] + aw3[30+c] : 0.f;
+    }
+    int np = t >> 3, kg = t & 7;
+    int n0 = np*2, n1 = np*2 + 1;
+    int kbase = kg*12 + (kg < 4 ? kg : 4);
+    int klen  = kg < 4 ? 13 : 12;
+    float a0[13], a1[13];
+#pragma unroll
+    for (int j = 0; j < 13; ++j) { a0[j] = 0.f; a1[j] = 0.f; }
+    for (int ch = 0; ch < 4; ++ch) {
+      __syncthreads();
+      for (int idx = t; idx < 4000; idx += 256) {
+        int r = idx/100, j = idx%100;
+        Wl[r*100 + j] = Wfc[(ch*40 + r)*100 + j];
+      }
+      __syncthreads();
+      for (int kk = 0; kk < 40; ++kk) {
+        float f0 = feat[n0*160 + ch*40+kk];
+        float f1 = feat[n1*160 + ch*40+kk];
+#pragma unroll
+        for (int j = 0; j < 13; ++j) {
+          if (j < klen) {
+            float w = Wl[kk*100 + kbase + j];
+            a0[j] += f0*w; a1[j] += f1*w;
+          }
+        }
+      }
+    }
+    __syncthreads();
+    float* sRow = shm;
+    for (int j = 0; j < klen; ++j) {
+      int k = kbase + j;
+      sRow[n0*100 + k] = a0[j] + bfc[k];
+      sRow[n1*100 + k] = a1[j] + bfc[k];
+    }
+    __syncthreads();
+    int n = t >> 2, part = t & 3;
+    int i0 = part*25;
+    float m = -3.4e38f;
+    for (int i = 0; i < 25; ++i) m = fmaxf(m, sRow[n*100 + i0 + i]);
+    m = fmaxf(m, __shfl_xor(m, 1));
+    m = fmaxf(m, __shfl_xor(m, 2));
+    float ev[25]; float s = 0.f;
+    for (int i = 0; i < 25; ++i) { float e = __expf(sRow[n*100 + i0 + i] - m); ev[i] = e; s += e; }
+    s += __shfl_xor(s, 1);
+    s += __shfl_xor(s, 2);
+    float rinv = 1.f / s;
+    for (int i = 0; i < 25; ++i) S[(size_t)(g0+n)*104 + i0 + i] = f2h(ev[i] * rinv);
+    if (part == 3) {
+      S[(size_t)(g0+n)*104 + 100] = 0; S[(size_t)(g0+n)*104 + 101] = 0;
+      S[(size_t)(g0+n)*104 + 102] = 0; S[(size_t)(g0+n)*104 + 103] = 0;
+    }
+  }
+  gridbar(cnt, 7*NBLK);
+
+  for (int vb = blk; vb < 832; vb += NBLK) {
+    int gid = vb * 256 + t;
     int row = gid / 13, q = gid - row*13;
     int len = rowlen[row];
     const float4* ev = (const float4*)(ellv + (size_t)row * CAP);
     const uint2*  ec = (const uint2*) (ellc + (size_t)row * CAP);
-    const uint4* HP = (const uint4*)(Hb100 + (size_t)(row >> 11) * ((size_t)NN*104));
+    const uint4* HP = (const uint4*)(S + (size_t)(row >> 11) * ((size_t)NN*104));
     float acc[8] = {0,0,0,0,0,0,0,0};
     int nit = len >> 2;
     for (int i = 0; i < nit; ++i) {
@@ -247,480 +533,227 @@
       uint2 cc = ec[i];
       int c0 = cc.x & 0xffff, c1 = cc.x >> 16, c2 = cc.y & 0xffff, c3 = cc.y >> 16;
       uint4 g0 = HP[c0*13+q], g1 = HP[c1*13+q], g2 = HP[c2*13+q], g3 = HP[c3*13+q];
-      float w0 = (v.x>0.f?1.f:0.f), w1 = (v.y>0.f?1.f:0.f);
-      float w2 = (v.z>0.f?1.f:0.f), w3 = (v.w>0.f?1.f:0.f);
-      ACC8(g0, w0); ACC8(g1, w1); ACC8(g2, w2); ACC8(g3, w3);
-    }
-    uint4 hs = HP[(row & (NN-1))*13 + q];
-    ACC8(hs, 1.f);
-    float d = dinvb[row];
-#pragma unroll
-    for (int k = 0; k < 8; ++k) acc[k] *= d;
-    float* Zp = Zb + (size_t)row*104 + q*8;
+      ACC8(g0, v.x); ACC8(g1, v.y); ACC8(g2, v.z); ACC8(g3, v.w);
+    }
+    float* Zp = As + (size_t)row*104 + q*8;
     float4 o0 = {acc[0],acc[1],acc[2],acc[3]}, o1 = {acc[4],acc[5],acc[6],acc[7]};
     ((float4*)Zp)[0] = o0; ((float4*)Zp)[1] = o1;
-    int c0 = q*8;
-#pragma unroll
-    for (int k = 0; k < 8; ++k) {
-      int ch = c0 + k;
-      if (ch < 100) { atomicAdd(&st[ch*2], acc[k]); atomicAdd(&st[ch*2+1], acc[k]*acc[k]); }
-    }
-    __syncthreads();
-    int copy = bid & 7;
-    for (int i = t; i < 200; i += 256)
-      atomicAdd(&bktB3[((i>>1)*8 + copy)*2 + (i&1)], st[i]);
-  }
-}
-
-template<int LEVEL>
-__global__ __launch_bounds__(256) void k_apply_gemm(
-    const float* __restrict__ Zw, const float* __restrict__ bktW,
-    const float* __restrict__ gW, const float* __restrict__ beW,
-    float* __restrict__ xst, const float* __restrict__ Ww,
-    const float* __restrict__ dinvw,
-    const float* __restrict__ Zb, const float* __restrict__ bktB,
-    const float* __restrict__ gB, const float* __restrict__ beB,
-    float* __restrict__ sst, const float* __restrict__ Wb,
-    const float* __restrict__ dinvb,
-    unsigned short* __restrict__ HwOut, unsigned short* __restrict__ HbOut)
-{
-  constexpr int NGB = (LEVEL == 1) ? 8 : 26;
-  constexpr int OSTRIDEB = (LEVEL == 1) ? 32 : 104;
-  constexpr int NG = 8 + NGB;
-  __shared__ float WwL[30*32];
-  __shared__ float WbL[30*OSTRIDEB];
-  __shared__ float awL[60], abL[60];
-  int t = threadIdx.x;
-  if (t < 60) {
-    int c = t % 30;
-    bool isW = t < 30;
-    const float4* p = (const float4*)((isW ? bktW : bktB) + c*128);
-    float s1 = 0.f, s2 = 0.f;
-#pragma unroll
-    for (int k = 0; k < 32; ++k) { float4 v = p[k]; s1 += v.x + v.z; s2 += v.y + v.w; }
-    float mean = s1/16384.f, var = s2/16384.f - mean*mean, inv = rsqrtf(var + 1e-5f);
-    float aa = (isW ? gW : gB)[c]*inv;
-    float* dst = isW ? awL : abL;
-    dst[c] = aa; dst[30+c] = (isW ? beW : beB)[c] - mean*aa;
-  }
-  for (int idx = t; idx < 30*32; idx += 256) {
-    int k = idx >> 5, c = idx & 31;
-    WwL[idx] = (c < 30) ? Ww[k*30 + c] : 0.f;
-  }
-  if (LEVEL == 1) {
-    for (int idx = t; idx < 30*32; idx += 256) {
-      int k = idx >> 5, c = idx & 31;
-      WbL[idx] = (c < 30) ? Wb[k*30 + c] : 0.f;
-    }
-  } else {
-    for (int idx = t; idx < 30*OSTRIDEB; idx += 256) {
-      int k = idx / OSTRIDEB, j = idx % OSTRIDEB;
-      WbL[idx] = (j < 100) ? Wb[k*100 + j] : 0.f;
-    }
-  }
-  __syncthreads();
-  int gid = blockIdx.x * 256 + t;
-  int row = gid / NG, g = gid % NG;
-  if (g < 8) {
-    const float4* Z4 = (const float4*)Zw + (size_t)row*8;
-    float4 z4[8];
-#pragma unroll
-    for (int u = 0; u < 8; ++u) z4[u] = Z4[u];
-    const float* z = (const float*)z4;
-    float4 xv;
-    int ch = 4*g;
-    xv.x = (ch+0 < 30) ? awL[ch+0]*z[ch+0] + awL[30+ch+0] : 0.f;
-    xv.y = (ch+1 < 30) ? awL[ch+1]*z[ch+1] + awL[30+ch+1] : 0.f;
-    xv.z = (ch+2 < 30) ? awL[ch+2]*z[ch+2] + awL[30+ch+2] : 0.f;
-    xv.w = (ch+3 < 30) ? awL[ch+3]*z[ch+3] + awL[30+ch+3] : 0.f;
-    ((float4*)xst)[(size_t)row*8+g] = xv;
-    float4 o = {0,0,0,0};
-#pragma unroll
-    for (int k = 0; k < 30; ++k) {
-      float xk = awL[k]*z[k] + awL[30+k];
-      float4 w = *(const float4*)(WwL + k*32 + 4*g);
-      FMA4(o, xk, w);
-    }
-    float d = dinvw[row];
-    us4 pv = { f2h(d*o.x), f2h(d*o.y), f2h(d*o.z), f2h(d*o.w) };
-    unsigned short* dst = (LEVEL == 1) ? (HwOut + (size_t)row*64 + 4*g)
-                                       : (HwOut + (size_t)row*32 + 4*g);
-    *(us4*)dst = pv;
-  } else {
-    int gb = g - 8;
-    const float4* Z4 = (const float4*)Zb + (size_t)row*8;
-    float4 z4[8];
-#pragma unroll
-    for (int u = 0; u < 8; ++u) z4[u] = Z4[u];
-    const float* z = (const float*)z4;
-    if (gb < 8) {
-      int ch = 4*gb;
-      float4 sv;
-      sv.x = (ch+0 < 30) ? abL[ch+0]*z[ch+0] + abL[30+ch+0] : 0.f;
-      sv.y = (ch+1 < 30) ? abL[ch+1]*z[ch+1] + abL[30+ch+1] : 0.f;
-      sv.z = (ch+2 < 30) ? abL[ch+2]*z[ch+2] + abL[30+ch+2] : 0.f;
-      sv.w = (ch+3 < 30) ? abL[ch+3]*z[ch+3] + abL[30+ch+3] : 0.f;
-      ((float4*)sst)[(size_t)row*8+gb] = sv;
-    }
-    float4 o = {0,0,0,0};
-#pragma unroll
-    for (int k = 0; k < 30; ++k) {
-      float sk = abL[k]*z[k] + abL[30+k];
-      float4 w = *(const float4*)(WbL + k*OSTRIDEB + 4*gb);
-      FMA4(o, sk, w);
-    }
-    float d = dinvb[row];
-    us4 pv = { f2h(d*o.x), f2h(d*o.y), f2h(d*o.z), f2h(d*o.w) };
-    unsigned short* dst = (LEVEL == 1) ? (HbOut + (size_t)row*64 + 32 + 4*gb)
-                                       : (HbOut + (size_t)row*104 + 4*gb);
-    *(us4*)dst = pv;
-  }
-}
-
-__global__ __launch_bounds__(256) void k_fcpool(
-    const float* __restrict__ Zw3, const float* __restrict__ bktW3,
-    const float* __restrict__ gW3, const float* __restrict__ beW3,
-    const float* __restrict__ Zb3, const float* __restrict__ bktB3,
-    const float* __restrict__ g100, const float* __restrict__ be100,
-    const float* __restrict__ s11, const float* __restrict__ s12,
-    const float* __restrict__ Wfc, const float* __restrict__ bfc,
-    float* __restrict__ x13, unsigned short* __restrict__ S)
-{
-  __shared__ float shm[14240];
-  __shared__ float aw3[60], ab3[200];
-  float* feat = shm;
-  float* Wl = shm + 10240;
-  int t = threadIdx.x;
-  int g0 = blockIdx.x * 64;
-  if (t < 30) {
-    const float4* p = (const float4*)(bktW3 + t*16);
-    float s1 = 0.f, s2 = 0.f;
-#pragma unroll
-    for (int k = 0; k < 4; ++k) { float4 v = p[k]; s1 += v.x + v.z; s2 += v.y + v.w; }
-    float mean = s1/16384.f, var = s2/16384.f - mean*mean, inv = rsqrtf(var + 1e-5f);
-    float aa = gW3[t]*inv; aw3[t] = aa; aw3[30+t] = beW3[t] - mean*aa;
-  } else if (t >= 64 && t < 164) {
-    int c = t - 64;
-    const float4* p = (const float4*)(bktB3 + c*16);
-    float s1 = 0.f, s2 = 0.f;
-#pragma unroll
-    for (int k = 0; k < 4; ++k) { float4 v = p[k]; s1 += v.x + v.z; s2 += v.y + v.w; }
-    float mean = s1/16384.f, var = s2/16384.f - mean*mean, inv = rsqrtf(var + 1e-5f);
-    float aa = g100[c]*inv; ab3[c] = aa; ab3[100+c] = be100[c] - mean*aa;
-  }
-  __syncthreads();
-  for (int idx = t; idx < 64*160; idx += 256) {
-    int l = idx / 160, c = idx % 160;
-    int g = g0 + l;
-    float v;
-    if (c < 30) v = s11[(size_t)g*32 + c];
-    else if (c < 60) v = s12[(size_t)g*32 + (c-30)];
-    else { int k = c - 60; v = ab3[k]*Zb3[(size_t)g*104 + k] + ab3[100 + k]; }
-    feat[l*160 + c] = v;
-  }
-  for (int idx = t; idx < 64*32; idx += 256) {
-    int l = idx >> 5, c = idx & 31;
-    int g = g0 + l;
-    x13[(size_t)g*32+c] = (c < 30) ? aw3[c]*Zw3[(size_t)g*32+c] + aw3[30+c] : 0.f;
-  }
-  int np = t >> 3, kg = t & 7;
-  int n0 = np*2, n1 = np*2 + 1;
-  int kbase = kg*12 + (kg < 4 ? kg : 4);
-  int klen  = kg < 4 ? 13 : 12;
-  float a0[13], a1[13];
-#pragma unroll
-  for (int j = 0; j < 13; ++j) { a0[j] = 0.f; a1[j] = 0.f; }
-  for (int ch = 0; ch < 4; ++ch) {
-    __syncthreads();
-    for (int idx = t; idx < 4000; idx += 256) {
-      int r = idx/100, j = idx%100;
-      Wl[r*100 + j] = Wfc[(ch*40 + r)*100 + j];
-    }
-    __syncthreads();
-    for (int kk = 0; kk < 40; ++kk) {
-      float f0 = feat[n0*160 + ch*40+kk];
-      float f1 = feat[n1*160 + ch*40+kk];
-#pragma unroll
-      for (int j = 0; j < 13; ++j) {
-        if (j < klen) {
-          float w = Wl[kk*100 + kbase + j];
-          a0[j] += f0*w; a1[j] += f1*w;
-        }
-      }
-    }
-  }
-  __syncthreads();
-  float* sRow = shm;
-  for (int j = 0; j < klen; ++j) {
-    int k = kbase + j;
-    sRow[n0*100 + k] = a0[j] + bfc[k];
-    sRow[n1*100 + k] = a1[j] + bfc[k];
-  }
-  __syncthreads();
-  int n = t >> 2, part = t & 3;
-  int i0 = part*25;
-  float m = -3.4e38f;
-  for (int i = 0; i < 25; ++i) m = fmaxf(m, sRow[n*100 + i0 + i]);
-  m = fmaxf(m, __shfl_xor(m, 1));
-  m = fmaxf(m, __shfl_xor(m, 2));
-  float ev[25]; float s = 0.f;
-  for (int i = 0; i < 25; ++i) { float e = __expf(sRow[n*100 + i0 + i] - m); ev[i] = e; s += e; }
-  s += __shfl_xor(s, 1);
-  s += __shfl_xor(s, 2);
-  float rinv = 1.f / s;
-  for (int i = 0; i < 25; ++i) S[(size_t)(g0+n)*104 + i0 + i] = f2h(ev[i] * rinv);
-  if (part == 3) {
-    S[(size_t)(g0+n)*104 + 100] = 0; S[(size_t)(g0+n)*104 + 101] = 0;
-    S[(size_t)(g0+n)*104 + 102] = 0; S[(size_t)(g0+n)*104 + 103] = 0;
-  }
-}
-
-__global__ __launch_bounds__(256) void k_spmm_as(
-    const unsigned short* __restrict__ S, const float* __restrict__ ellv,
-    const unsigned short* __restrict__ ellc, const int* __restrict__ rowlen,
-    float* __restrict__ Z)
-{
-  int t = threadIdx.x;
-  int gid = blockIdx.x * 256 + t;
-  int row = gid / 13, q = gid - row*13;
-  int len = rowlen[row];
-  const float4* ev = (const float4*)(ellv + (size_t)row * CAP);
-  const uint2*  ec = (const uint2*) (ellc + (size_t)row * CAP);
-  const uint4* HP = (const uint4*)(S + (size_t)(row >> 11) * ((size_t)NN*104));
-  float acc[8] = {0,0,0,0,0,0,0,0};
-  int nit = len >> 2;
-  for (int i = 0; i < nit; ++i) {
-    float4 v = ev[i];
-    uint2 cc = ec[i];
-    int c0 = cc.x & 0xffff, c1 = cc.x >> 16, c2 = cc.y & 0xffff, c3 = cc.y >> 16;
-    uint4 g0 = HP[c0*13+q], g1 = HP[c1*13+q], g2 = HP[c2*13+q], g3 = HP[c3*13+q];
-    ACC8(g0, v.x); ACC8(g1, v.y); ACC8(g2, v.z); ACC8(g3, v.w);
-  }
-  float* Zp = Z + (size_t)row*104 + q*8;
-  float4 o0 = {acc[0],acc[1],acc[2],acc[3]}, o1 = {acc[4],acc[5],acc[6],acc[7]};
-  ((float4*)Zp)[0] = o0; ((float4*)Zp)[1] = o1;
-}
-
-__global__ __launch_bounds__(256) void k_pool_part(
-    const unsigned short* __restrict__ S, const float* __restrict__ x13,
-    const float* __restrict__ As, const float* __restrict__ x11,
-    const float* __restrict__ x12, float* __restrict__ pp, float* __restrict__ pm)
-{
-  __shared__ float sL[64][100];
-  __shared__ float xL[64][132];
-  __shared__ float red[256];
-  int t = threadIdx.x;
-  int b = blockIdx.x >> 3, chunk = blockIdx.x & 7;
-  int g00 = b * 2048 + chunk * 256;
-  int kt = t/10, dt = t%10;
-  int k0 = kt*4, d0 = dt*13;
-  float acc[4][13];
-#pragma unroll
-  for (int a = 0; a < 4; ++a)
-#pragma unroll
-    for (int j = 0; j < 13; ++j) acc[a][j] = 0.f;
-  for (int tile = 0; tile < 4; ++tile) {
-    int g0 = g00 + tile*64;
-    __syncthreads();
-    for (int idx = t; idx < 64*100; idx += 256) {
-      int l = idx/100, k = idx%100;
-      sL[l][k] = h2f(S[(size_t)(g0+l)*104 + k]);
-    }
-    for (int idx = t; idx < 64*130; idx += 256) {
-      int l = idx/130, d = idx%130;
-      xL[l][d] = d < 30 ? x13[(size_t)(g0+l)*32 + d] : As[(size_t)(g0+l)*104 + (d-30)];
-    }
-    __syncthreads();
+  }
+  gridbar(cnt, 8*NBLK);
+
+  if (blk < 64) {
+    float* sL = shm;
+    float* xL = shm + 6400;
+    float* red = shm + 14848;
+    int b = blk >> 3, chunk = blk & 7;
+    int g00 = b * 2048 + chunk * 256;
+    int kt = t/10, dt = t%10;
+    int k0 = kt*4, d0 = dt*13;
+    float acc[4][13];
+#pragma unroll
+    for (int a = 0; a < 4; ++a)
+#pragma unroll
+      for (int j = 0; j < 13; ++j) acc[a][j] = 0.f;
+    for (int tile = 0; tile < 4; ++tile) {
+      int g0 = g00 + tile*64;
+      __syncthreads();
+      for (int idx = t; idx < 64*100; idx += 256) {
+        int l = idx/100, k = idx%100;
+        sL[l*100 + k] = h2f(S[(size_t)(g0+l)*104 + k]);
+      }
+      for (int idx = t; idx < 64*130; idx += 256) {
+        int l = idx/130, d = idx%130;
+        xL[l*132 + d] = d < 30 ? x13[(size_t)(g0+l)*32 + d] : As[(size_t)(g0+l)*104 + (d-30)];
+      }
+      __syncthreads();
+      if (t < 250) {
+        for (int kk = 0; kk < 64; ++kk) {
+          float sv[4];
+#pragma unroll
+          for (int a = 0; a < 4; ++a) sv[a] = sL[kk*100 + k0+a];
+#pragma unroll
+          for (int j = 0; j < 13; ++j) {
+            float xv = xL[kk*132 + d0+j];
+#pragma unroll
+            for (int a = 0; a < 4; ++a) acc[a][j] += sv[a]*xv;
+          }
+        }
+      }
+    }
     if (t < 250) {
-      for (int kk = 0; kk < 64; ++kk) {
-        float sv[4];
-#pragma unroll
-        for (int a = 0; a < 4; ++a) sv[a] = sL[kk][k0+a];
-#pragma unroll
-        for (int j = 0; j < 13; ++j) {
-          float xv = xL[kk][d0+j];
-#pragma unroll
-          for (int a = 0; a < 4; ++a) acc[a][j] += sv[a]*xv;
-        }
-      }
-    }
-  }
-  if (t < 250) {
-    float* dst = pp + (size_t)blockIdx.x * 13000;
-    for (int a = 0; a < 4; ++a)
-      for (int j = 0; j < 13; ++j)
-        dst[(k0+a)*130 + (d0+j)] = acc[a][j];
-  }
-  __syncthreads();
+      float* dst = pp + (size_t)blk * 13000;
+      for (int a = 0; a < 4; ++a)
+        for (int j = 0; j < 13; ++j)
+          dst[(k0+a)*130 + (d0+j)] = acc[a][j];
+    }
+    __syncthreads();
+    {
+      int c = t & 31, rg = t >> 5;
+      const float* srcs[3] = {x11, x12, x13};
+      for (int a = 0; a < 3; ++a) {
+        const float* p = srcs[a] + (size_t)(g00+rg)*32 + c;
+        float m = -3.4e38f;
+        for (int it = 0; it < 32; ++it) m = fmaxf(m, p[it*256]);
+        red[t] = m;
+        __syncthreads();
+        if (t < 30) {
+          float mm = red[t];
+          for (int g = 1; g < 8; ++g) mm = fmaxf(mm, red[g*32+t]);
+          partmax[(size_t)blk*90 + a*30 + t] = mm;
+        }
+        __syncthreads();
+      }
+    }
+  }
+  gridbar(cnt, 9*NBLK);
+
+  if (blk >= 8) return;
+
   {
-    int c = t & 31, rg = t >> 5;
-    const float* srcs[3] = {x11, x12, x13};
-    for (int a = 0; a < 3; ++a) {
-      const float* p = srcs[a] + (size_t)(g00+rg)*32 + c;
+    float* A2f  = shm;
+    float* buf1 = shm + 10000;
+    float* buf2 = shm + 13000;
+    float* WL   = shm + 16200;
+    float* dl   = shm + 17160;
+    float* st1  = shm + 17260;
+    float* st2  = shm + 17290;
+    float* coef = shm + 17320;
+    float* x1L  = shm + 17380;
+    float* x2L  = shm + 17470;
+    float* hh   = shm + 17560;
+    int b = blk;
+    __syncthreads();
+    for (int idx = t; idx < 13000; idx += 256) {
+      float s = 0.f;
+      for (int ch = 0; ch < 8; ++ch) s += pp[(size_t)(b*8 + ch)*13000 + idx];
+      int k = idx/130, d = idx%130;
+      if (d < 30) buf1[k*30 + d] = s;
+      else A2f[k*100 + (d-30)] = s;
+    }
+    __syncthreads();
+    if (t < 100 && A2f[t*101] == 0.f) A2f[t*101] = 1.f;
+    __syncthreads();
+    if (t < 100) {
+      float s = 0.f;
+      for (int j = 0; j < 100; ++j) s += A2f[t*100 + j];
+      dl[t] = s > 0.f ? rsqrtf(s) : 0.f;
+    }
+    __syncthreads();
+    for (int idx = t; idx < 10000; idx += 256) {
+      int i = idx/100, j = idx%100;
+      A2f[idx] = dl[i]*dl[j]*A2f[idx];
+    }
+    int rp = t >> 2, cg = t & 3;
+    int i0 = rp*2, c0 = cg*8;
+    bool act = (t < 200);
+    for (int L = 0; L < 3; ++L) {
+      if (t < 30) { st1[t] = 0.f; st2[t] = 0.f; }
+      const float* W = W3030 + 3*900 + L*900;
+      for (int idx = t; idx < 960; idx += 256) {
+        int k = idx >> 5, c = idx & 31;
+        WL[idx] = (c < 30) ? W[k*30 + c] : 0.f;
+      }
+      __syncthreads();
+      if (act) {
+        float a0[8] = {0,0,0,0,0,0,0,0}, a1[8] = {0,0,0,0,0,0,0,0};
+        for (int k = 0; k < 30; ++k) {
+          float xx0 = buf1[i0*30 + k], xx1 = buf1[(i0+1)*30 + k];
+          float4 w0 = *(const float4*)&WL[k*32 + c0];
+          float4 w1 = *(const float4*)&WL[k*32 + c0 + 4];
+          a0[0] += xx0*w0.x; a0[1] += xx0*w0.y; a0[2] += xx0*w0.z; a0[3] += xx0*w0.w;
+          a0[4] += xx0*w1.x; a0[5] += xx0*w1.y; a0[6] += xx0*w1.z; a0[7] += xx0*w1.w;
+          a1[0] += xx1*w0.x; a1[1] += xx1*w0.y; a1[2] += xx1*w0.z; a1[3] += xx1*w0.w;
+          a1[4] += xx1*w1.x; a1[5] += xx1*w1.y; a1[6] += xx1*w1.z; a1[7] += xx1*w1.w;
+        }
+        float4 s00 = {a0[0],a0[1],a0[2],a0[3]}, s01 = {a0[4],a0[5],a0[6],a0[7]};
+        float4 s10 = {a1[0],a1[1],a1[2],a1[3]}, s11v = {a1[4],a1[5],a1[6],a1[7]};
+        *(float4*)&buf2[i0*32 + c0]       = s00;
+        *(float4*)&buf2[i0*32 + c0 + 4]   = s01;
+        *(float4*)&buf2[(i0+1)*32 + c0]   = s10;
+        *(float4*)&buf2[(i0+1)*32 + c0+4] = s11v;
+      }
+      __syncthreads();
+      if (act) {
+        float z0[8] = {0,0,0,0,0,0,0,0}, z1[8] = {0,0,0,0,0,0,0,0};
+        for (int j = 0; j < 100; ++j) {
+          float av0 = A2f[i0*100 + j], av1 = A2f[(i0+1)*100 + j];
+          float4 t0 = *(const float4*)&buf2[j*32 + c0];
+          float4 t1 = *(const float4*)&buf2[j*32 + c0 + 4];
+          z0[0] += av0*t0.x; z0[1] += av0*t0.y; z0[2] += av0*t0.z; z0[3] += av0*t0.w;
+          z0[4] += av0*t1.x; z0[5] += av0*t1.y; z0[6] += av0*t1.z; z0[7] += av0*t1.w;
+          z1[0] += av1*t0.x; z1[1] += av1*t0.y; z1[2] += av1*t0.z; z1[3] += av1*t0.w;
+          z1[4] += av1*t1.x; z1[5] += av1*t1.y; z1[6] += av1*t1.z; z1[7] += av1*t1.w;
+        }
+#pragma unroll
+        for (int k = 0; k < 8; ++k) {
+          int c = c0 + k;
+          if (c < 30) {
+            buf1[i0*30 + c]     = z0[k];
+            buf1[(i0+1)*30 + c] = z1[k];
+            atomicAdd(&st1[c], z0[k] + z1[k]);
+            atomicAdd(&st2[c], z0[k]*z0[k] + z1[k]*z1[k]);
+          }
+        }
+      }
+      __syncthreads();
+      if (t < 30) {
+        atomicAdd(&bktS2[(L*30+t)*2],   st1[t]);
+        atomicAdd(&bktS2[(L*30+t)*2+1], st2[t]);
+      }
+      __syncthreads();
+      if (t == 0) {
+        __threadfence();
+        atomicAdd(cnt2, 1);
+        while (atomicAdd(cnt2, 0) < (L+1)*8) {}
+        __threadfence();
+      }
+      __syncthreads();
+      if (t < 30) {
+        float s1 = atomicAdd(&bktS2[(L*30+t)*2],   0.f);
+        float s2 = atomicAdd(&bktS2[(L*30+t)*2+1], 0.f);
+        float mean = s1/800.f, var = s2/800.f - mean*mean, inv = rsqrtf(var + 1e-5f);
+        float aa = g30[150+L*30+t]*inv;
+        coef[t] = aa; coef[30+t] = be30[150+L*30+t] - mean*aa;
+      }
+      __syncthreads();
+      if (L < 2) {
+        for (int idx = t; idx < 3000; idx += 256) {
+          int c = idx % 30;
+          buf1[idx] = coef[c]*buf1[idx] + coef[30+c];
+        }
+        __syncthreads();
+        if (t < 30) {
+          float m = -3.4e38f;
+          for (int i = 0; i < 100; ++i) m = fmaxf(m, buf1[i*30+t]);
+          x2L[L*30+t] = m;
+        }
+        __syncthreads();
+      } else {
+        if (t < 30) {
+          float m = -3.4e38f;
+          for (int i = 0; i < 100; ++i) m = fmaxf(m, coef[t]*buf1[i*30+t] + coef[30+t]);
+          x2L[60+t] = m;
+        }
+      }
+    }
+    if (t < 90) {
       float m = -3.4e38f;
-      for (int it = 0; it < 32; ++it) m = fmaxf(m, p[it*256]);
-      red[t] = m;
-      __syncthreads();
-      if (t < 30) {
-        float mm = red[t];
-        for (int g = 1; g < 8; ++g) mm = fmaxf(mm, red[g*32+t]);
-        pm[(size_t)blockIdx.x*90 + a*30 + t] = mm;
-      }
-      __syncthreads();
-    }
-  }
-}
-
-__global__ __launch_bounds__(256) void k_s2fused(
-    const float* __restrict__ pp, const float* __restrict__ partmax,
-    const float* __restrict__ Wm,
-    const float* __restrict__ g30,
-    const float* __restrict__ be30,
-    float* __restrict__ bktS2,
-    int* __restrict__ cnt,
-    const float* __restrict__ W1, const float* __restrict__ b1,
-    const float* __restrict__ W2, const float* __restrict__ b2,
-    float* __restrict__ out)
-{
-  __shared__ float A2f[10000];
-  __shared__ float buf1[3000];
-  __shared__ float buf2[3200];
-  __shared__ float WL[960];
-  __shared__ float dl[100];
-  __shared__ float st1[30], st2[30];
-  __shared__ float coef[60];
-  __shared__ float x1L[90], x2L[90], hh[50];
-  int b = blockIdx.x, t = threadIdx.x;
-  for (int idx = t; idx < 13000; idx += 256) {
-    float s = 0.f;
-    for (int ch = 0; ch < 8; ++ch) s += pp[(size_t)(b*8 + ch)*13000 + idx];
-    int k = idx/130, d = idx%130;
-    if (d < 30) buf1[k*30 + d] = s;
-    else A2f[k*100 + (d-30)] = s;
-  }
-  __syncthreads();
-  if (t < 100 && A2f[t*101] == 0.f) A2f[t*101] = 1.f;
-  __syncthreads();
-  if (t < 100) {
-    float s = 0.f;
-    for (int j = 0; j < 100; ++j) s += A2f[t*100 + j];
-    dl[t] = s > 0.f ? rsqrtf(s) : 0.f;
-  }
-  __syncthreads();
-  for (int idx = t; idx < 10000; idx += 256) {
-    int i = idx/100, j = idx%100;
-    A2f[idx] = dl[i]*dl[j]*A2f[idx];
-  }
-  int rp = t >> 2, cg = t & 3;
-  int i0 = rp*2, c0 = cg*8;
-  bool act = (t < 200);
-  for (int L = 0; L < 3; ++L) {
-    if (t < 30) { st1[t] = 0.f; st2[t] = 0.f; }
-    const float* W = Wm + L*900;
-    for (int idx = t; idx < 960; idx += 256) {
-      int k = idx >> 5, c = idx & 31;
-      WL[idx] = (c < 30) ? W[k*30 + c] : 0.f;
-    }
-    __syncthreads();
-    if (act) {
-      float a0[8] = {0,0,0,0,0,0,0,0}, a1[8] = {0,0,0,0,0,0,0,0};
-      for (int k = 0; k < 30; ++k) {
-        float xx0 = buf1[i0*30 + k], xx1 = buf1[(i0+1)*30 + k];
-        float4 w0 = *(const float4*)&WL[k*32 + c0];
-        float4 w1 = *(const float4*)&WL[k*32 + c0 + 4];
-        a0[0] += xx0*w0.x; a0[1] += xx0*w0.y; a0[2] += xx0*w0.z; a0[3] += xx0*w0.w;
-        a0[4] += xx0*w1.x; a0[5] += xx0*w1.y; a0[6] += xx0*w1.z; a0[7] += xx0*w1.w;
-        a1[0] += xx1*w0.x; a1[1] += xx1*w0.y; a1[2] += xx1*w0.z; a1[3] += xx1*w0.w;
-        a1[4] += xx1*w1.x; a1[5] += xx1*w1.y; a1[6] += xx1*w1.z; a1[7] += xx1*w1.w;
-      }
-      float4 s00 = {a0[0],a0[1],a0[2],a0[3]}, s01 = {a0[4],a0[5],a0[6],a0[7]};
-      float4 s10 = {a1[0],a1[1],a1[2],a1[3]}, s11v = {a1[4],a1[5],a1[6],a1[7]};
-      *(float4*)&buf2[i0*32 + c0]       = s00;
-      *(float4*)&buf2[i0*32 + c0 + 4]   = s01;
-      *(float4*)&buf2[(i0+1)*32 + c0]   = s10;
-      *(float4*)&buf2[(i0+1)*32 + c0+4] = s11v;
-    }
-    __syncthreads();
-    if (act) {
-      float z0[8] = {0,0,0,0,0,0,0,0}, z1[8] = {0,0,0,0,0,0,0,0};
-      for (int j = 0; j < 100; ++j) {
-        float av0 = A2f[i0*100 + j], av1 = A2f[(i0+1)*100 + j];
-        float4 t0 = *(const float4*)&buf2[j*32 + c0];
-        float4 t1 = *(const float4*)&buf2[j*32 + c0 + 4];
-        z0[0] += av0*t0.x; z0[1] += av0*t0.y; z0[2] += av0*t0.z; z0[3] += av0*t0.w;
-        z0[4] += av0*t1.x; z0[5] += av0*t1.y; z0[6] += av0*t1.z; z0[7] += av0*t1.w;
-        z1[0] += av1*t0.x; z1[1] += av1*t0.y; z1[2] += av1*t0.z; z1[3] += av1*t0.w;
-        z1[4] += av1*t1.x; z1[5] += av1*t1.y; z1[6] += av1*t1.z; z1[7] += av1*t1.w;
-      }
-#pragma unroll
-      for (int k = 0; k < 8; ++k) {
-        int c = c0 + k;
-        if (c < 30) {
-          buf1[i0*30 + c]     = z0[k];
-          buf1[(i0+1)*30 + c] = z1[k];
-          atomicAdd(&st1[c], z0[k] + z1[k]);
-          atomicAdd(&st2[c], z0[k]*z0[k] + z1[k]*z1[k]);
-        }
-      }
-    }
-    __syncthreads();
-    if (t < 30) {
-      atomicAdd(&bktS2[(L*30+t)*2],   st1[t]);
-      atomicAdd(&bktS2[(L*30+t)*2+1], st2[t]);
-    }
-    __syncthreads();
-    if (t == 0) {
-      __threadfence();
-      atomicAdd(cnt, 1);
-      while (atomicAdd(cnt, 0) < (L+1)*8) {}
-      __threadfence();
-    }
-    __syncthreads();
-    if (t < 30) {
-      float s1 = atomicAdd(&bktS2[(L*30+t)*2],   0.f);
-      float s2 = atomicAdd(&bktS2[(L*30+t)*2+1], 0.f);
-      float mean = s1/800.f, var = s2/800.f - mean*mean, inv = rsqrtf(var + 1e-5f);
-      float aa = g30[L*30+t]*inv;
-      coef[t] = aa; coef[30+t] = be30[L*30+t] - mean*aa;
-    }
-    __syncthreads();
-    if (L < 2) {
-      for (int idx = t; idx < 3000; idx += 256) {
-        int c = idx % 30;
-        buf1[idx] = coef[c]*buf1[idx] + coef[30+c];
-      }
-      __syncthreads();
-      if (t < 30) {
-        float m = -3.4e38f;
-        for (int i = 0; i < 100; ++i) m = fmaxf(m, buf1[i*30+t]);
-        x2L[L*30+t] = m;
-      }
-      __syncthreads();
-    } else {
-      if (t < 30) {
-        float m = -3.4e38f;
-        for (int i = 0; i < 100; ++i) m = fmaxf(m, coef[t]*buf1[i*30+t] + coef[30+t]);
-        x2L[60+t] = m;
-      }
-    }
-  }
-  if (t < 90) {
-    float m = -3.4e38f;
-    for (int s = 0; s < 8; ++s) m = fmaxf(m, partmax[(size_t)(b*8+s)*90 + t]);
-    x1L[t] = m;
-  }
-  __syncthreads();
-  if (t < 50) {
-    float a = b1[t];
-    for (int k = 0; k < 90; ++k) a += x1L[k]*W1[k*50+t];
-    for (int k = 0; k < 90; ++k) a += x2L[k]*W1[(90+k)*50+t];
-    hh[t] = fmaxf(a, 0.f);
-  }
-  __syncthreads();
-  if (t < 6) {
-    float a = b2[t];
-    for (int j = 0; j < 50; ++j) a += hh[j]*W2[j*6+t];
-    out[b*6+t] = a;
+      for (int s = 0; s < 8; ++s) m = fmaxf(m, partmax[(size_t)(b*8+s)*90 + t]);
+      x1L[t] = m;
+    }
+    __syncthreads();
+    if (t < 50) {
+      float a = b1[t];
+      for (int k = 0; k < 90; ++k) a += x1L[k]*W1[k*50+t];
+      for (int k = 0; k < 90; ++k) a += x2L[k]*W1[(90+k)*50+t];
+      hh[t] = fmaxf(a, 0.f);
+    }
+    __syncthreads();
+    if (t < 6) {
+      float a = b2[t];
+      for (int j = 0; j < 50; ++j) a += hh[j]*W2[j*6+t];
+      out[b*6+t] = a;
+    }
   }
 }
 
@@ -743,50 +776,10 @@
   const float* be30 = (const float*)d_in[14];
   const float* g100 = (const float*)d_in[15];
   const float* be100= (const float*)d_in[16];
-  float* out = (float*)d_out;
-
   float* wsf = (float*)d_ws;
-  float* bL1W = wsf + OF_B1W;  float* bL1B = wsf + OF_B1B;
-  float* bL2W = wsf + OF_B2W;  float* bL2B = wsf + OF_B2B;
-  float* bL3W = wsf + OF_B3W;  float* bL3B = wsf + OF_B3B;
-  float* bktS2 = wsf + OF_S2;
-  int*   cnt  = (int*)(wsf + OF_CNT);
-  float* ellv  = wsf + OF_ELLV;
-  unsigned short* ellc = (unsigned short*)(wsf + OF_ELLC);
-  int*   rowlen = (int*)(wsf + OF_ROWLEN);
-  float* dinvw = wsf + OF_DINVW;
-  float* dinvb = wsf + OF_DINVB;
-  unsigned short* Hwb   = (unsigned short*)(wsf + OF_HWB);
-  unsigned short* Hw3   = (unsigned short*)(wsf + OF_HW3);
-  unsigned short* Hb100 = (unsigned short*)(wsf + OF_HB100);
-  unsigned short* S     = Hb100;
-  float* Zw = wsf + OF_ZW;
-  float* Zb = wsf + OF_ZB;
-  float* x11 = wsf + OF_X11;
-  float* x12 = wsf + OF_X12;
-  float* x13 = wsf + OF_X13;
-  float* s11 = wsf + OF_S11;
-  float* s12 = wsf + OF_S12;
-  float* pp  = wsf + OF_S11;
-  float* partmax = wsf + OF_PARTMAX;
-
-  k_build_ell<<<RTOT, 256, 0, stream>>>(adj, x, Win, ellv, ellc, rowlen, dinvw, dinvb, Hwb, wsf);
-
-  k_spmm_pair<<<512, 256, 0, stream>>>(Hwb, ellv, ellc, rowlen, dinvw, dinvb, Zw, Zb, bL1W, bL1B);
-  k_apply_gemm<1><<<1024, 256, 0, stream>>>(Zw, bL1W, g30+0, be30+0, x11, W3030+0, dinvw,
-                                            Zb, bL1B, g30+90, be30+90, s11, W3030+2*900, dinvb, Hwb, Hwb);
-
-  k_spmm_pair<<<512, 256, 0, stream>>>(Hwb, ellv, ellc, rowlen, dinvw, dinvb, Zw, Zb, bL2W, bL2B);
-  k_apply_gemm<2><<<2176, 256, 0, stream>>>(Zw, bL2W, g30+30, be30+30, x12, W3030+900, dinvw,
-                                            Zb, bL2B, g30+120, be30+120, s12, Wp13, dinvb, Hw3, Hb100);
-
-  k_spmm_l3<<<1088, 256, 0, stream>>>(Hw3, Hb100, ellv, ellc, rowlen, dinvw, dinvb, Zw, Zb, bL3W, bL3B);
-  k_fcpool<<<256, 256, 0, stream>>>(Zw, bL3W, g30+60, be30+60, Zb, bL3B, g100, be100,
-                                    s11, s12, Wfc, bfc, x13, S);
-
-  k_spmm_as<<<832, 256, 0, stream>>>(S, ellv, ellc, rowlen, Zb );
-  k_pool_part<<<64, 256, 0, stream>>>(S, x13, Zb, x11, x12, pp, partmax);
-
-  k_s2fused<<<BATCH, 256, 0, stream>>>(pp, partmax, W3030+3*900, g30+150, be30+150,
-                                       bktS2, cnt, W1, b1, W2, b2, out);
+
+  hipMemsetAsync(wsf, 0, ZEND * sizeof(float), stream);
+  k_mega<<<NBLK, 256, 0, stream>>>(adj, x, Win, W3030, Wp13, Wfc, bfc,
+                                   W1, b1, W2, b2, g30, be30, g100, be100,
+                                   wsf, (float*)d_out);
 }
```

Result: slower. 1.220 ms (+86.0%).
